# Kernel tuning notes

Hardware: AMD Instinct MI355X
Metric: run time of the kernel (lower is better)

## Reference

```python
import jax, jax.numpy as jnp
import numpy as np

N_TASK = 50000
N_EDGE = 50000
E = 500000
F_TASK = 64
F_EDGE = 64
H = 256
OUT = 256


def _lin(key, fan_in, fan_out):
    kw, kb = jax.random.split(key)
    lim = 1.0 / np.sqrt(fan_in)
    W = jax.random.uniform(kw, (fan_in, fan_out), minval=-lim, maxval=lim, dtype=jnp.float32)
    b = jax.random.uniform(kb, (fan_out,), minval=-lim, maxval=lim, dtype=jnp.float32)
    return W, b


def setup_inputs() -> dict:
    key = jax.random.key(0)
    ks = jax.random.split(key, 20)
    inp = {}
    inp['task_features'] = jax.random.normal(ks[0], (N_TASK, F_TASK), dtype=jnp.float32)
    inp['edge_features'] = jax.random.normal(ks[1], (N_EDGE, F_EDGE), dtype=jnp.float32)
    inp['queue_edges'] = jax.random.randint(ks[2], (2, E), 0, N_TASK)
    inp['type_edges'] = jax.random.randint(ks[3], (2, E), 0, N_TASK)
    inp['affinity_edges'] = jax.random.randint(ks[4], (2, E), 0, N_TASK)  # src<num_tasks, tgt<num_edges
    inp['topology_edges'] = jax.random.randint(ks[5], (2, E), 0, N_EDGE)
    inp['te_w1'], inp['te_b1'] = _lin(ks[6], F_TASK, H)
    inp['te_w2'], inp['te_b2'] = _lin(ks[7], H, H)
    inp['ee_w1'], inp['ee_b1'] = _lin(ks[8], F_EDGE, H)
    inp['ee_w2'], inp['ee_b2'] = _lin(ks[9], H, H)
    inp['gnn_w0'], inp['gnn_b0'] = _lin(ks[10], H, H)
    inp['gnn_w1'], inp['gnn_b1'] = _lin(ks[11], H, H)
    inp['ta_w'], inp['ta_b'] = _lin(ks[12], H, H)
    inp['ea_w'], inp['ea_b'] = _lin(ks[13], H, H)
    inp['out_w1'], inp['out_b1'] = _lin(ks[14], 2 * H, H)
    inp['out_w2'], inp['out_b2'] = _lin(ks[15], H, OUT)
    return inp


def _mean_msg(src_emb, src, tgt, num_segments):
    # scatter-add messages from src nodes into tgt slots, divide by in-degree (clamped >=1)
    msgs = jax.ops.segment_sum(src_emb[src], tgt, num_segments=num_segments)
    cnt = jax.ops.segment_sum(jnp.ones_like(src, dtype=src_emb.dtype), tgt, num_segments=num_segments)
    return msgs / jnp.maximum(cnt, 1.0)[:, None]


def _forward(task_features, edge_features, queue_edges, type_edges, affinity_edges, topology_edges,
             te_w1, te_b1, te_w2, te_b2, ee_w1, ee_b1, ee_w2, ee_b2,
             gnn_w0, gnn_b0, gnn_w1, gnn_b1, ta_w, ta_b, ea_w, ea_b,
             out_w1, out_b1, out_w2, out_b2):
    relu = jax.nn.relu
    # node encoders (Linear-ReLU-Linear-ReLU)
    t = relu(relu(task_features @ te_w1 + te_b1) @ te_w2 + te_b2)   # [N_task, H]
    e = relu(relu(edge_features @ ee_w1 + ee_b1) @ ee_w2 + ee_b2)   # [N_edge, H]

    # queue convolution: messages computed ONCE from original t (torch code never updates task_embeddings in loop)
    qs, qt = queue_edges[0], queue_edges[1]
    q_msgs = jax.ops.segment_sum(t[qs], qt, num_segments=t.shape[0])
    h = t
    for W, b in ((gnn_w0, gnn_b0), (gnn_w1, gnn_b1)):
        h = relu((h + 0.5 * q_msgs) @ W + b)
    t = h

    # type convolution: mean-aggregated same-type messages
    t = t + 0.3 * _mean_msg(t, type_edges[0], type_edges[1], t.shape[0])

    # affinity convolution: bipartite task<->edge exchange (simultaneous update)
    asrc, atgt = affinity_edges[0], affinity_edges[1]
    t_msgs = jax.ops.segment_sum(e[atgt], asrc, num_segments=t.shape[0])
    t_cnt = jax.ops.segment_sum(jnp.ones((asrc.shape[0],), t.dtype), asrc, num_segments=t.shape[0])
    e_msgs = jax.ops.segment_sum(t[asrc], atgt, num_segments=e.shape[0])
    e_cnt = jax.ops.segment_sum(jnp.ones((atgt.shape[0],), e.dtype), atgt, num_segments=e.shape[0])
    t_new = t + 0.3 * t_msgs / jnp.maximum(t_cnt, 1.0)[:, None]
    e_new = e + 0.3 * e_msgs / jnp.maximum(e_cnt, 1.0)[:, None]
    t, e = t_new, e_new

    # topology convolution: edge-edge mean aggregation
    e = e + 0.3 * _mean_msg(e, topology_edges[0], topology_edges[1], e.shape[0])

    # graph-level aggregation
    t_agg = relu(jnp.mean(t, axis=0) @ ta_w + ta_b)  # [H]
    e_agg = relu(jnp.mean(e, axis=0) @ ea_w + ea_b)  # [H]
    combined = jnp.concatenate([t_agg, e_agg], axis=0)  # [2H]
    out = relu(combined @ out_w1 + out_b1) @ out_w2 + out_b2  # [OUT]
    return out


def reference(task_features, edge_features, queue_edges, type_edges, affinity_edges, topology_edges,
              te_w1, te_b1, te_w2, te_b2, ee_w1, ee_b1, ee_w2, ee_b2,
              gnn_w0, gnn_b0, gnn_w1, gnn_b1, ta_w, ta_b, ea_w, ea_b,
              out_w1, out_b1, out_w2, out_b2):
    return _forward(task_features, edge_features, queue_edges, type_edges, affinity_edges, topology_edges,
                    te_w1, te_b1, te_w2, te_b2, ee_w1, ee_b1, ee_w2, ee_b2,
                    gnn_w0, gnn_b0, gnn_w1, gnn_b1, ta_w, ta_b, ea_w, ea_b,
                    out_w1, out_b1, out_w2, out_b2)
```

## Files before the change

kernel.cpp:

```cpp
#include <hip/hip_runtime.h>

#define H 256
#define NT 50000
#define NEDGE 50000
#define NE 500000

#define NBKT 391
#define NBLK 123
#define CHUNK 4096
#define CAP 2816

typedef __attribute__((ext_vector_type(8))) short short8_t;
typedef __attribute__((ext_vector_type(4))) float f32x4;
typedef unsigned short u16;
typedef unsigned int u32;

__device__ __forceinline__ float b2f(u16 v) { return __uint_as_float((u32)v << 16); }
__device__ __forceinline__ u16 f2b(float f) {
    u32 u = __float_as_uint(f);
    u += 0x7FFFu + ((u >> 16) & 1u);
    return (u16)(u >> 16);
}

__device__ __forceinline__ u32 f2fp8_1(float f) {
    u32 u = __float_as_uint(f);
    u32 s = (u >> 24) & 0x80u;
    float af = fabsf(f);
    if (af >= 448.f) return s | 0x7Eu;
    if (af < 0.015625f) {
        int m = (int)rintf(af * 512.0f);
        return s | (u32)m;
    }
    u32 au = __float_as_uint(af);
    u32 r = au + 0x7FFFFu + ((au >> 20) & 1u);
    int e = (int)(r >> 23) - 127;
    return s | (u32)(((e + 7) << 3) | ((r >> 20) & 7u));
}
__device__ __forceinline__ float fp82f_1(u32 b) {
    u32 s = (b & 0x80u) << 24;
    u32 em = b & 0x7Fu;
    float v;
    if (em >= 8) v = __uint_as_float((((em >> 3) + 120u) << 23) | ((em & 7u) << 20));
    else v = (float)em * 0.001953125f;
    return __uint_as_float(__float_as_uint(v) | s);
}
__device__ __forceinline__ u32 pk4_fp8(float a, float b, float c, float d) {
#if __has_builtin(__builtin_amdgcn_cvt_pk_fp8_f32)
    u32 r = 0;
    r = (u32)__builtin_amdgcn_cvt_pk_fp8_f32(a, b, (int)r, false);
    r = (u32)__builtin_amdgcn_cvt_pk_fp8_f32(c, d, (int)r, true);
    return r;
#else
    return f2fp8_1(a) | (f2fp8_1(b) << 8) | (f2fp8_1(c) << 16) | (f2fp8_1(d) << 24);
#endif
}
__device__ __forceinline__ float4 unpk4_fp8(u32 v) {
#if __has_builtin(__builtin_amdgcn_cvt_pk_f32_fp8)
    auto lo = __builtin_amdgcn_cvt_pk_f32_fp8(v, false);
    auto hi = __builtin_amdgcn_cvt_pk_f32_fp8(v, true);
    return make_float4(lo[0], lo[1], hi[0], hi[1]);
#else
    return make_float4(fp82f_1(v & 255u), fp82f_1((v >> 8) & 255u),
                       fp82f_1((v >> 16) & 255u), fp82f_1(v >> 24));
#endif
}

__device__ __forceinline__ const int* pick_list(
    int l, const int* a, const int* b, const int* c, const int* d, const int* e)
{ return (l == 0) ? a : (l == 1) ? b : (l == 2) ? c : (l == 3) ? d : e; }

template<int K1, bool XF32, bool DUAL>
__global__ __launch_bounds__(256) void fused_mlp(
    const void* __restrict__ XA,
    const u16* __restrict__ W1hA, const u16* __restrict__ W1lA, const float* __restrict__ b1A,
    const u16* __restrict__ W2hA, const u16* __restrict__ W2lA, const float* __restrict__ b2A,
    u16* __restrict__ outA, u32* __restrict__ f8A,
    const void* __restrict__ XB,
    const u16* __restrict__ W1hB, const u16* __restrict__ W1lB, const float* __restrict__ b1B,
    const u16* __restrict__ W2hB, const u16* __restrict__ W2lB, const float* __restrict__ b2B,
    u16* __restrict__ outB, u32* __restrict__ f8B,
    int N, int nA)
{
    __shared__ u16 lds[64 * 256];
    int bid = blockIdx.x;
    const void* X = XA;
    const u16 *W1h = W1hA, *W1l = W1lA, *W2h = W2hA, *W2l = W2lA;
    const float *b1 = b1A, *b2 = b2A;
    u16* out = outA;
    u32* f8 = f8A;
    if (DUAL && bid >= nA) {
        bid -= nA; X = XB;
        W1h = W1hB; W1l = W1lB; b1 = b1B;
        W2h = W2hB; W2l = W2lB; b2 = b2B;
        out = outB; f8 = f8B;
    }
    const int m0 = bid * 64;

    constexpr int RCH = K1 / 8;
    for (int i = threadIdx.x; i < 64 * RCH; i += 256) {
        int r = i / RCH, c8 = i % RCH;
        int gr = m0 + r; if (gr >= N) gr = N - 1;
        uint4 v;
        if (XF32) {
            const float* xf = (const float*)X + (size_t)gr * K1 + c8 * 8;
            float4 a = *(const float4*)xf;
            float4 b = *(const float4*)(xf + 4);
            v.x = (u32)f2b(a.x) | ((u32)f2b(a.y) << 16);
            v.y = (u32)f2b(a.z) | ((u32)f2b(a.w) << 16);
            v.z = (u32)f2b(b.x) | ((u32)f2b(b.y) << 16);
            v.w = (u32)f2b(b.z) | ((u32)f2b(b.w) << 16);
        } else {
            v = *(const uint4*)((const u16*)X + (size_t)gr * K1 + c8 * 8);
        }
        u32 byte = (u32)(r * (K1 * 2) + c8 * 16) ^ (u32)((r & 7) << 4);
        *(uint4*)((char*)lds + byte) = v;
    }
    __syncthreads();

    const int wv = threadIdx.x >> 6, l = threadIdx.x & 63;
    const int li = l & 15, lk = l >> 4;

    f32x4 acc[4][4];
    #pragma unroll
    for (int i = 0; i < 4; i++)
        #pragma unroll
        for (int j = 0; j < 4; j++)
            acc[i][j] = (f32x4){0.f, 0.f, 0.f, 0.f};

    {
        constexpr int KS = K1 / 32;
        short8_t whc[4], wlc[4];
        #pragma unroll
        for (int ni = 0; ni < 4; ni++) {
            const size_t wi = (size_t)((wv * 4 + ni) * KS) * 64 + l;
            whc[ni] = ((const short8_t*)W1h)[wi];
            wlc[ni] = ((const short8_t*)W1l)[wi];
        }
        #pragma unroll
        for (int ks = 0; ks < KS; ks++) {
            short8_t whn[4], wln[4];
            if (ks + 1 < KS) {
                #pragma unroll
                for (int ni = 0; ni < 4; ni++) {
                    const size_t wi = (size_t)((wv * 4 + ni) * KS + ks + 1) * 64 + l;
                    whn[ni] = ((const short8_t*)W1h)[wi];
                    wln[ni] = ((const short8_t*)W1l)[wi];
                }
            }
            short8_t xb[4];
            #pragma unroll
            for (int mi = 0; mi < 4; mi++) {
                int m = mi * 16 + li;
                u32 byte = (u32)(m * (K1 * 2) + (ks * 32 + lk * 8) * 2) ^ (u32)((m & 7) << 4);
                xb[mi] = *(const short8_t*)((const char*)lds + byte);
            }
            __builtin_amdgcn_s_setprio(1);
            #pragma unroll
            for (int ni = 0; ni < 4; ni++)
                #pragma unroll
                for (int mi = 0; mi < 4; mi++) {
                    acc[mi][ni] = __builtin_amdgcn_mfma_f32_16x16x32_bf16(wlc[ni], xb[mi], acc[mi][ni], 0, 0, 0);
                    acc[mi][ni] = __builtin_amdgcn_mfma_f32_16x16x32_bf16(whc[ni], xb[mi], acc[mi][ni], 0, 0, 0);
                }
            __builtin_amdgcn_s_setprio(0);
            if (ks + 1 < KS) {
                #pragma unroll
                for (int ni = 0; ni < 4; ni++) { whc[ni] = whn[ni]; wlc[ni] = wln[ni]; }
            }
        }
    }

    __syncthreads();

    #pragma unroll
    for (int ni = 0; ni < 4; ni++) {
        int c = wv * 64 + ni * 16 + lk * 4;
        float4 b4 = *(const float4*)(b1 + c);
        #pragma unroll
        for (int mi = 0; mi < 4; mi++) {
            int m = mi * 16 + li;
            float o0 = fmaxf(acc[mi][ni][0] + b4.x, 0.f);
            float o1 = fmaxf(acc[mi][ni][1] + b4.y, 0.f);
            float o2 = fmaxf(acc[mi][ni][2] + b4.z, 0.f);
            float o3 = fmaxf(acc[mi][ni][3] + b4.w, 0.f);
            u32 w0 = (u32)f2b(o0) | ((u32)f2b(o1) << 16);
            u32 w1 = (u32)f2b(o2) | ((u32)f2b(o3) << 16);
            u32 byte = (u32)(m * 512 + c * 2) ^ (u32)((m & 7) << 4);
            *(uint2*)((char*)lds + byte) = make_uint2(w0, w1);
        }
    }
    __syncthreads();

    #pragma unroll
    for (int i = 0; i < 4; i++)
        #pragma unroll
        for (int j = 0; j < 4; j++)
            acc[i][j] = (f32x4){0.f, 0.f, 0.f, 0.f};

    {
        short8_t whc[4], wlc[4];
        #pragma unroll
        for (int ni = 0; ni < 4; ni++) {
            const size_t wi = (size_t)((wv * 4 + ni) * 8) * 64 + l;
            whc[ni] = ((const short8_t*)W2h)[wi];
            wlc[ni] = ((const short8_t*)W2l)[wi];
        }
        #pragma unroll
        for (int ks = 0; ks < 8; ks++) {
            short8_t whn[4], wln[4];
            if (ks + 1 < 8) {
                #pragma unroll
                for (int ni = 0; ni < 4; ni++) {
                    const size_t wi = (size_t)((wv * 4 + ni) * 8 + ks + 1) * 64 + l;
                    whn[ni] = ((const short8_t*)W2h)[wi];
                    wln[ni] = ((const short8_t*)W2l)[wi];
                }
            }
            short8_t xb[4];
            #pragma unroll
            for (int mi = 0; mi < 4; mi++) {
                int m = mi * 16 + li;
                u32 byte = (u32)(m * 512 + (ks * 32 + lk * 8) * 2) ^ (u32)((m & 7) << 4);
                xb[mi] = *(const short8_t*)((const char*)lds + byte);
            }
            __builtin_amdgcn_s_setprio(1);
            #pragma unroll
            for (int ni = 0; ni < 4; ni++)
                #pragma unroll
                for (int mi = 0; mi < 4; mi++) {
                    acc[mi][ni] = __builtin_amdgcn_mfma_f32_16x16x32_bf16(wlc[ni], xb[mi], acc[mi][ni], 0, 0, 0);
                    acc[mi][ni] = __builtin_amdgcn_mfma_f32_16x16x32_bf16(whc[ni], xb[mi], acc[mi][ni], 0, 0, 0);
                }
            __builtin_amdgcn_s_setprio(0);
            if (ks + 1 < 8) {
                #pragma unroll
                for (int ni = 0; ni < 4; ni++) { whc[ni] = whn[ni]; wlc[ni] = wln[ni]; }
            }
        }
    }

    #pragma unroll
    for (int mi = 0; mi < 4; mi++) {
        int m = m0 + mi * 16 + li;
        if (m < N) {
            #pragma unroll
            for (int ni = 0; ni < 4; ni++) {
                int c = wv * 64 + ni * 16 + lk * 4;
                float4 b4 = *(const float4*)(b2 + c);
                float o0 = fmaxf(acc[mi][ni][0] + b4.x, 0.f);
                float o1 = fmaxf(acc[mi][ni][1] + b4.y, 0.f);
                float o2 = fmaxf(acc[mi][ni][2] + b4.z, 0.f);
                float o3 = fmaxf(acc[mi][ni][3] + b4.w, 0.f);
                u32 w0 = (u32)f2b(o0) | ((u32)f2b(o1) << 16);
                u32 w1 = (u32)f2b(o2) | ((u32)f2b(o3) << 16);
                *(uint2*)(out + (size_t)m * H + c) = make_uint2(w0, w1);
                if (f8) f8[(size_t)m * 64 + (c >> 2)] = pk4_fp8(o0, o1, o2, o3);
            }
        }
    }
}

__global__ __launch_bounds__(256) void gnn_fused(
    const u16* __restrict__ T, const u32* __restrict__ M0,
    const int* __restrict__ csr, const int* __restrict__ off,
    const u16* __restrict__ W1h, const u16* __restrict__ W1l, const float* __restrict__ b1,
    const u16* __restrict__ W2h, const u16* __restrict__ W2l, const float* __restrict__ b2,
    u16* __restrict__ out, u32* __restrict__ f8, int N)
{
    __shared__ u16 ldsX[64 * 256];
    __shared__ u16 ldsS[64 * 256];
    const int wv = threadIdx.x >> 6, l = threadIdx.x & 63;
    const int li = l & 15, lk = l >> 4;
    const int m0 = blockIdx.x * 64;

    for (int rr = 0; rr < 16; rr++) {
        int r = wv * 16 + rr;
        int gr = m0 + r; if (gr >= N) gr = N - 1;
        int o0 = off[gr];
        int d  = off[gr + 1] - o0;
        float4 acc = {0.f, 0.f, 0.f, 0.f};
        int j = 0;
        for (; j + 8 <= d; j += 8) {
            u32 w[8];
            #pragma unroll
            for (int q = 0; q < 8; q++)
                w[q] = M0[(size_t)csr[o0 + j + q] * 64 + l];
            #pragma unroll
            for (int q = 0; q < 8; q++) {
                float4 f = unpk4_fp8(w[q]);
                acc.x += f.x; acc.y += f.y; acc.z += f.z; acc.w += f.w;
            }
        }
        for (; j < d; j++) {
            float4 f = unpk4_fp8(M0[(size_t)csr[o0 + j] * 64 + l]);
            acc.x += f.x; acc.y += f.y; acc.z += f.z; acc.w += f.w;
        }
        ushort4 t4 = ((const ushort4*)(T + (size_t)gr * H))[l];
        u32 s0 = (u32)f2b(acc.x) | ((u32)f2b(acc.y) << 16);
        u32 s1 = (u32)f2b(acc.z) | ((u32)f2b(acc.w) << 16);
        u32 f0 = (u32)f2b(fmaf(0.5f, acc.x, b2f(t4.x)))
               | ((u32)f2b(fmaf(0.5f, acc.y, b2f(t4.y))) << 16);
        u32 f1 = (u32)f2b(fmaf(0.5f, acc.z, b2f(t4.z)))
               | ((u32)f2b(fmaf(0.5f, acc.w, b2f(t4.w))) << 16);
        u32 byte = (u32)(r * 512 + l * 8) ^ (u32)((r & 7) << 4);
        *(uint2*)((char*)ldsX + byte) = make_uint2(f0, f1);
        *(uint2*)((char*)ldsS + byte) = make_uint2(s0, s1);
    }
    __syncthreads();

    f32x4 acc[4][4];
    #pragma unroll
    for (int i = 0; i < 4; i++)
        #pragma unroll
        for (int j = 0; j < 4; j++)
            acc[i][j] = (f32x4){0.f, 0.f, 0.f, 0.f};

    {
        short8_t whc[4], wlc[4];
        #pragma unroll
        for (int ni = 0; ni < 4; ni++) {
            const size_t wi = (size_t)((wv * 4 + ni) * 8) * 64 + l;
            whc[ni] = ((const short8_t*)W1h)[wi];
            wlc[ni] = ((const short8_t*)W1l)[wi];
        }
        #pragma unroll
        for (int ks = 0; ks < 8; ks++) {
            short8_t whn[4], wln[4];
            if (ks + 1 < 8) {
                #pragma unroll
                for (int ni = 0; ni < 4; ni++) {
                    const size_t wi = (size_t)((wv * 4 + ni) * 8 + ks + 1) * 64 + l;
                    whn[ni] = ((const short8_t*)W1h)[wi];
                    wln[ni] = ((const short8_t*)W1l)[wi];
                }
            }
            short8_t xb[4];
            #pragma unroll
            for (int mi = 0; mi < 4; mi++) {
                int m = mi * 16 + li;
                u32 byte = (u32)(m * 512 + (ks * 32 + lk * 8) * 2) ^ (u32)((m & 7) << 4);
                xb[mi] = *(const short8_t*)((const char*)ldsX + byte);
            }
            __builtin_amdgcn_s_setprio(1);
            #pragma unroll
            for (int ni = 0; ni < 4; ni++)
                #pragma unroll
                for (int mi = 0; mi < 4; mi++) {
                    acc[mi][ni] = __builtin_amdgcn_mfma_f32_16x16x32_bf16(wlc[ni], xb[mi], acc[mi][ni], 0, 0, 0);
                    acc[mi][ni] = __builtin_amdgcn_mfma_f32_16x16x32_bf16(whc[ni], xb[mi], acc[mi][ni], 0, 0, 0);
                }
            __builtin_amdgcn_s_setprio(0);
            if (ks + 1 < 8) {
                #pragma unroll
                for (int ni = 0; ni < 4; ni++) { whc[ni] = whn[ni]; wlc[ni] = wln[ni]; }
            }
        }
    }

    __syncthreads();

    #pragma unroll
    for (int ni = 0; ni < 4; ni++) {
        int c = wv * 64 + ni * 16 + lk * 4;
        float4 b4 = *(const float4*)(b1 + c);
        #pragma unroll
        for (int mi = 0; mi < 4; mi++) {
            int m = mi * 16 + li;
            u32 byte = (u32)(m * 512 + c * 2) ^ (u32)((m & 7) << 4);
            uint2 sv = *(const uint2*)((const char*)ldsS + byte);
            float o0 = fmaxf(acc[mi][ni][0] + b4.x, 0.f);
            float o1 = fmaxf(acc[mi][ni][1] + b4.y, 0.f);
            float o2 = fmaxf(acc[mi][ni][2] + b4.z, 0.f);
            float o3 = fmaxf(acc[mi][ni][3] + b4.w, 0.f);
            o0 = fmaf(0.5f, b2f((u16)(sv.x & 0xFFFF)), o0);
            o1 = fmaf(0.5f, b2f((u16)(sv.x >> 16)), o1);
            o2 = fmaf(0.5f, b2f((u16)(sv.y & 0xFFFF)), o2);
            o3 = fmaf(0.5f, b2f((u16)(sv.y >> 16)), o3);
            u32 w0 = (u32)f2b(o0) | ((u32)f2b(o1) << 16);
            u32 w1 = (u32)f2b(o2) | ((u32)f2b(o3) << 16);
            *(uint2*)((char*)ldsX + byte) = make_uint2(w0, w1);
        }
    }
    __syncthreads();

    #pragma unroll
    for (int i = 0; i < 4; i++)
        #pragma unroll
        for (int j = 0; j < 4; j++)
            acc[i][j] = (f32x4){0.f, 0.f, 0.f, 0.f};

    {
        short8_t whc[4], wlc[4];
        #pragma unroll
        for (int ni = 0; ni < 4; ni++) {
            const size_t wi = (size_t)((wv * 4 + ni) * 8) * 64 + l;
            whc[ni] = ((const short8_t*)W2h)[wi];
            wlc[ni] = ((const short8_t*)W2l)[wi];
        }
        #pragma unroll
        for (int ks = 0; ks < 8; ks++) {
            short8_t whn[4], wln[4];
            if (ks + 1 < 8) {
                #pragma unroll
                for (int ni = 0; ni < 4; ni++) {
                    const size_t wi = (size_t)((wv * 4 + ni) * 8 + ks + 1) * 64 + l;
                    whn[ni] = ((const short8_t*)W2h)[wi];
                    wln[ni] = ((const short8_t*)W2l)[wi];
                }
            }
            short8_t xb[4];
            #pragma unroll
            for (int mi = 0; mi < 4; mi++) {
                int m = mi * 16 + li;
                u32 byte = (u32)(m * 512 + (ks * 32 + lk * 8) * 2) ^ (u32)((m & 7) << 4);
                xb[mi] = *(const short8_t*)((const char*)ldsX + byte);
            }
            __builtin_amdgcn_s_setprio(1);
            #pragma unroll
            for (int ni = 0; ni < 4; ni++)
                #pragma unroll
                for (int mi = 0; mi < 4; mi++) {
                    acc[mi][ni] = __builtin_amdgcn_mfma_f32_16x16x32_bf16(wlc[ni], xb[mi], acc[mi][ni], 0, 0, 0);
                    acc[mi][ni] = __builtin_amdgcn_mfma_f32_16x16x32_bf16(whc[ni], xb[mi], acc[mi][ni], 0, 0, 0);
                }
            __builtin_amdgcn_s_setprio(0);
            if (ks + 1 < 8) {
                #pragma unroll
                for (int ni = 0; ni < 4; ni++) { whc[ni] = whn[ni]; wlc[ni] = wln[ni]; }
            }
        }
    }

    #pragma unroll
    for (int mi = 0; mi < 4; mi++) {
        int m = m0 + mi * 16 + li;
        if (m < N) {
            #pragma unroll
            for (int ni = 0; ni < 4; ni++) {
                int c = wv * 64 + ni * 16 + lk * 4;
                float4 b4 = *(const float4*)(b2 + c);
                float o0 = fmaxf(acc[mi][ni][0] + b4.x, 0.f);
                float o1 = fmaxf(acc[mi][ni][1] + b4.y, 0.f);
                float o2 = fmaxf(acc[mi][ni][2] + b4.z, 0.f);
                float o3 = fmaxf(acc[mi][ni][3] + b4.w, 0.f);
                u32 w0 = (u32)f2b(o0) | ((u32)f2b(o1) << 16);
                u32 w1 = (u32)f2b(o2) | ((u32)f2b(o3) << 16);
                *(uint2*)(out + (size_t)m * H + c) = make_uint2(w0, w1);
                if (f8) f8[(size_t)m * 64 + (c >> 2)] = pk4_fp8(o0, o1, o2, o3);
            }
        }
    }
}

__global__ __launch_bounds__(256) void wt_pack(
    const float* __restrict__ s0, const float* __restrict__ s1,
    const float* __restrict__ s2, const float* __restrict__ s3,
    const float* __restrict__ s4, const float* __restrict__ s5,
    u16* __restrict__ arena)
{
    const int li = blockIdx.y;
    const int K = (li == 0 || li == 4) ? 64 : 256;
    const int offs[6] = {0, 32768, 163840, 294912, 425984, 458752};
    int n = K * 256;
    int i = blockIdx.x * 256 + threadIdx.x;
    if (i >= n) return;
    const float* W = (li == 0) ? s0 : (li == 1) ? s1 : (li == 2) ? s2
                   : (li == 3) ? s3 : (li == 4) ? s4 : s5;
    u16* hi = arena + offs[li];
    u16* lo = hi + n;
    int k = i >> 8, c = i & 255;
    float u = W[i];
    u32 b = __float_as_uint(u);
    float r = u - __uint_as_float(b & 0xFFFF0000u);
    int lane = ((k >> 3) & 3) * 16 + (c & 15);
    size_t idx = ((size_t)((c >> 4) * (K >> 5) + (k >> 5)) * 64 + lane) * 8 + (k & 7);
    hi[idx] = (u16)(b >> 16);
    lo[idx] = f2b(r);
}

__global__ __launch_bounds__(256) void hist_kernel(
    const int* __restrict__ k0, const int* __restrict__ k1, const int* __restrict__ k2,
    const int* __restrict__ k3, const int* __restrict__ k4, int* __restrict__ counts)
{
    __shared__ int h[NBKT];
    int l = blockIdx.y;
    const int* k = pick_list(l, k0, k1, k2, k3, k4);
    for (int i = threadIdx.x; i < NBKT; i += 256) h[i] = 0;
    __syncthreads();
    int e0 = blockIdx.x * CHUNK;
    for (int i = threadIdx.x; i < CHUNK; i += 256) {
        int e = e0 + i;
        if (e < NE) atomicAdd(&h[k[e] >> 7], 1);
    }
    __syncthreads();
    int* out = counts + ((size_t)l * NBLK + blockIdx.x) * NBKT;
    for (int i = threadIdx.x; i < NBKT; i += 256) out[i] = h[i];
}

__global__ __launch_bounds__(256) void scan_buckets(
    const int* __restrict__ counts, int* __restrict__ starts, int* __restrict__ bases)
{
    __shared__ int buf[256];
    int l = blockIdx.x, t = threadIdx.x;
    const int* cl = counts + (size_t)l * NBLK * NBKT;
    int* sl = starts + (size_t)l * NBLK * NBKT;
    int b0 = t * 2;
    int totloc[2];
    int s = 0;
    #pragma unroll
    for (int j = 0; j < 2; j++) {
        int b = b0 + j, v = 0;
        if (b < NBKT) for (int k = 0; k < NBLK; k++) v += cl[k * NBKT + b];
        totloc[j] = v; s += v;
    }
    buf[t] = s; __syncthreads();
    for (int st = 1; st < 256; st <<= 1) {
        int v = (t >= st) ? buf[t - st] : 0; __syncthreads();
        buf[t] += v; __syncthreads();
    }
    int run = buf[t] - s;
    #pragma unroll
    for (int j = 0; j < 2; j++) {
        int b = b0 + j;
        if (b < NBKT) {
            bases[l * (NBKT + 1) + b] = run;
            int p = run;
            for (int k = 0; k < NBLK; k++) { sl[k * NBKT + b] = p; p += cl[k * NBKT + b]; }
            run += totloc[j];
        }
    }
    if (t == 255) bases[l * (NBKT + 1) + NBKT] = NE;
}

__global__ __launch_bounds__(256) void partition_kernel(
    const int* __restrict__ k0, const int* __restrict__ k1, const int* __restrict__ k2,
    const int* __restrict__ k3, const int* __restrict__ k4,
    const int* __restrict__ v0, const int* __restrict__ v1, const int* __restrict__ v2,
    const int* __restrict__ v3, const int* __restrict__ v4,
    const int* __restrict__ starts, int* __restrict__ csr)
{
    __shared__ u32 ent[CHUNK];
    __shared__ u16 ebk[CHUNK];
    __shared__ int cnt[NBKT], loff[NBKT], cur[NBKT], gst[NBKT];
    __shared__ int buf[256];
    int l = blockIdx.y, t = threadIdx.x;
    const int* k = pick_list(l, k0, k1, k2, k3, k4);
    const int* v = pick_list(l, v0, v1, v2, v3, v4);
    const int* st = starts + ((size_t)l * NBLK + blockIdx.x) * NBKT;
    for (int i = t; i < NBKT; i += 256) { cnt[i] = 0; gst[i] = st[i]; }
    __syncthreads();
    int e0 = blockIdx.x * CHUNK;
    u32 ep[16]; int eb[16];
    #pragma unroll
    for (int j = 0; j < 16; j++) {
        int e = e0 + j * 256 + t;
        if (e < NE) {
            int key = k[e];
            eb[j] = key >> 7;
            ep[j] = ((u32)(key & 127) << 16) | (u32)v[e];
            atomicAdd(&cnt[eb[j]], 1);
        } else eb[j] = -1;
    }
    __syncthreads();
    int b0 = t * 2;
    int c0 = (b0 < NBKT) ? cnt[b0] : 0;
    int c1 = (b0 + 1 < NBKT) ? cnt[b0 + 1] : 0;
    int s = c0 + c1;
    buf[t] = s; __syncthreads();
    for (int stp = 1; stp < 256; stp <<= 1) {
        int x = (t >= stp) ? buf[t - stp] : 0; __syncthreads();
        buf[t] += x; __syncthreads();
    }
    int run = buf[t] - s;
    if (b0 < NBKT)     { loff[b0] = run;          cur[b0] = run; }
    if (b0 + 1 < NBKT) { loff[b0 + 1] = run + c0; cur[b0 + 1] = run + c0; }
    __syncthreads();
    #pragma unroll
    for (int j = 0; j < 16; j++) {
        if (eb[j] >= 0) {
            int p = atomicAdd(&cur[eb[j]], 1);
            ent[p] = ep[j]; ebk[p] = (u16)eb[j];
        }
    }
    __syncthreads();
    int nv = min(CHUNK, NE - e0);
    int* c = csr + (size_t)l * NE;
    for (int i = t; i < nv; i += 256) {
        int b = ebk[i];
        c[gst[b] + (i - loff[b])] = (int)ent[i];
    }
}

__global__ __launch_bounds__(256) void bucket_csr(
    const int* __restrict__ bases, int* __restrict__ csr, int* __restrict__ off)
{
    __shared__ int seg[CAP];
    __shared__ int hist[128], scn[128];
    int l = blockIdx.y, b = blockIdx.x, t = threadIdx.x;
    int base = bases[l * (NBKT + 1) + b];
    int end  = bases[l * (NBKT + 1) + b + 1];
    int sz = end - base; if (sz > CAP) sz = CAP;
    int* c = csr + (size_t)l * NE;
    for (int i = t; i < sz; i += 256) seg[i] = c[base + i];
    if (t < 128) hist[t] = 0;
    __syncthreads();
    for (int i = t; i < sz; i += 256) atomicAdd(&hist[seg[i] >> 16], 1);
    __syncthreads();
    if (t < 128) scn[t] = hist[t];
    __syncthreads();
    for (int st = 1; st < 128; st <<= 1) {
        int v = 0;
        if (t < 128 && t >= st) v = scn[t - st];
        __syncthreads();
        if (t < 128) scn[t] += v;
        __syncthreads();
    }
    if (t < 128) {
        int key = b * 128 + t;
        int excl = scn[t] - hist[t];
        if (key < NT) off[l * (NT + 1) + key] = base + excl;
        hist[t] = excl;
    }
    if (b == 0 && t == 128) off[l * (NT + 1) + NT] = NE;
    __syncthreads();
    for (int i = t; i < sz; i += 256) {
        int u = seg[i];
        int p = atomicAdd(&hist[u >> 16], 1);
        c[base + p] = u & 0xFFFF;
    }
}

__global__ __launch_bounds__(256) void gather_mean_f8(
    const u32* __restrict__ srcA, const int* __restrict__ csrA, const int* __restrict__ offA,
    const u16* __restrict__ baseA, u16* __restrict__ dstA, u32* __restrict__ m8A,
    const u32* __restrict__ srcB, const int* __restrict__ csrB, const int* __restrict__ offB,
    const u16* __restrict__ baseB, u16* __restrict__ dstB, u32* __restrict__ m8B,
    float alpha, int nA, int N)
{
    int bid = blockIdx.x;
    const u32* src = srcA; const int* csr = csrA; const int* off = offA;
    const u16* base = baseA; u16* dst = dstA; u32* m8 = m8A;
    if (bid >= nA) {
        bid -= nA; src = srcB; csr = csrB; off = offB; base = baseB; dst = dstB; m8 = m8B;
    }
    int r = (bid * 256 + threadIdx.x) >> 6;
    int lane = threadIdx.x & 63;
    if (r >= N) return;
    int o0 = off[r];
    int d  = off[r + 1] - o0;
    float4 acc = {0.f, 0.f, 0.f, 0.f};
    int j = 0;
    for (; j + 8 <= d; j += 8) {
        u32 w[8];
        #pragma unroll
        for (int q = 0; q < 8; q++)
            w[q] = src[(size_t)csr[o0 + j + q] * 64 + lane];
        #pragma unroll
        for (int q = 0; q < 8; q++) {
            float4 f = unpk4_fp8(w[q]);
            acc.x += f.x; acc.y += f.y; acc.z += f.z; acc.w += f.w;
        }
    }
    for (; j < d; j++) {
        float4 f = unpk4_fp8(src[(size_t)csr[o0 + j] * 64 + lane]);
        acc.x += f.x; acc.y += f.y; acc.z += f.z; acc.w += f.w;
    }
    float s = alpha / (float)max(d, 1);
    ushort4 b = ((const ushort4*)(base + (size_t)r * H))[lane];
    float o0f = fmaf(s, acc.x, b2f(b.x));
    float o1f = fmaf(s, acc.y, b2f(b.y));
    float o2f = fmaf(s, acc.z, b2f(b.z));
    float o3f = fmaf(s, acc.w, b2f(b.w));
    ushort4 pk;
    pk.x = f2b(o0f); pk.y = f2b(o1f); pk.z = f2b(o2f); pk.w = f2b(o3f);
    ((ushort4*)(dst + (size_t)r * H))[lane] = pk;
    if (m8) m8[(size_t)r * 64 + lane] = pk4_fp8(o0f, o1f, o2f, o3f);
}

__global__ __launch_bounds__(256) void colsum_slots(
    const u16* __restrict__ embA, const u16* __restrict__ embB,
    float* __restrict__ part, int N)
{
    int blk = blockIdx.x;
    const u16* emb = (blk < 256) ? embA : embB;
    int rb = blk & 255;
    int c = threadIdx.x;
    float s = 0.f;
    for (int r = rb; r < N; r += 256)
        s += b2f(emb[(size_t)r * H + c]);
    part[(size_t)blk * H + c] = s;
}

__global__ __launch_bounds__(256) void final_mlp(
    const float* __restrict__ part, float invNT, float invNE,
    const float* __restrict__ ta_w, const float* __restrict__ ta_b,
    const float* __restrict__ ea_w, const float* __restrict__ ea_b,
    const float* __restrict__ ow1, const float* __restrict__ ob1,
    const float* __restrict__ ow2, const float* __restrict__ ob2,
    float* __restrict__ out)
{
    __shared__ float tm[H], em[H], comb[2 * H], hid[H];
    int t = threadIdx.x;
    float st = 0.f, se = 0.f;
    for (int b = 0; b < 256; b++) {
        st += part[(size_t)b * H + t];
        se += part[(size_t)(256 + b) * H + t];
    }
    tm[t] = st * invNT;
    em[t] = se * invNE;
    __syncthreads();
    float s = ta_b[t];
    for (int k = 0; k < H; k++) s += tm[k] * ta_w[k * H + t];
    comb[t] = fmaxf(s, 0.f);
    s = ea_b[t];
    for (int k = 0; k < H; k++) s += em[k] * ea_w[k * H + t];
    comb[H + t] = fmaxf(s, 0.f);
    __syncthreads();
    s = ob1[t];
    for (int k = 0; k < 2 * H; k++) s += comb[k] * ow1[k * H + t];
    hid[t] = fmaxf(s, 0.f);
    __syncthreads();
    s = ob2[t];
    for (int k = 0; k < H; k++) s += hid[k] * ow2[k * H + t];
    out[t] = s;
}

extern "C" void kernel_launch(void* const* d_in, const int* in_sizes, int n_in,
                              void* d_out, int out_size, void* d_ws, size_t ws_size,
                              hipStream_t stream) {
    const float* tf  = (const float*)d_in[0];
    const float* ef  = (const float*)d_in[1];
    const int*   qe  = (const int*)d_in[2];
    const int*   te  = (const int*)d_in[3];
    const int*   ae  = (const int*)d_in[4];
    const int*   pe  = (const int*)d_in[5];
    const float* te_w1 = (const float*)d_in[6];  const float* te_b1 = (const float*)d_in[7];
    const float* te_w2 = (const float*)d_in[8];  const float* te_b2 = (const float*)d_in[9];
    const float* ee_w1 = (const float*)d_in[10]; const float* ee_b1 = (const float*)d_in[11];
    const float* ee_w2 = (const float*)d_in[12]; const float* ee_b2 = (const float*)d_in[13];
    const float* gw0 = (const float*)d_in[14];   const float* gb0 = (const float*)d_in[15];
    const float* gw1 = (const float*)d_in[16];   const float* gb1 = (const float*)d_in[17];
    const float* ta_w = (const float*)d_in[18];  const float* ta_b = (const float*)d_in[19];
    const float* ea_w = (const float*)d_in[20];  const float* ea_b = (const float*)d_in[21];
    const float* ow1 = (const float*)d_in[22];   const float* ob1 = (const float*)d_in[23];
    const float* ow2 = (const float*)d_in[24];   const float* ob2 = (const float*)d_in[25];

    const size_t NB = (size_t)NT * H;
    u16* T  = (u16*)d_ws;
    u16* Bf = T + NB;
    u16* S  = Bf + NB;
    u16* F  = S + NB;
    float* sumpad = (float*)(F + NB);
    int* off5   = (int*)(sumpad + 2 * H);
    int* csr5   = off5 + 5 * (NT + 1);
    int* counts = csr5 + (size_t)5 * NE;
    int* starts = counts + (size_t)5 * NBLK * NBKT;
    int* bases  = starts + (size_t)5 * NBLK * NBKT;
    u16* arena = (u16*)(((size_t)counts + 15) & ~(size_t)15);
    u16* wt_te1_h = arena + 0;      u16* wt_te1_l = arena + 16384;
    u16* wt_te2_h = arena + 32768;  u16* wt_te2_l = arena + 98304;
    u16* wt_g0_h  = arena + 163840; u16* wt_g0_l  = arena + 229376;
    u16* wt_g1_h  = arena + 294912; u16* wt_g1_l  = arena + 360448;
    u16* wt_ee1_h = arena + 425984; u16* wt_ee1_l = arena + 442368;
    u16* wt_ee2_h = arena + 458752; u16* wt_ee2_l = arena + 524288;
    u32* M0 = (u32*)(((size_t)(bases + 5 * (NBKT + 1)) + 15) & ~(size_t)15);
    u32* M1 = M0 + NB / 4;
    u32* M2 = M1 + NB / 4;
    u32* M3 = M2 + NB / 4;
    u32* M4 = M3 + NB / 4;
    float* part = (float*)(M4 + NB / 4);

    const int MG = (NT + 63) / 64;
    const int GB = (NT * 64) / 256;

    const int *k0 = qe + NE, *k1 = te + NE, *k2 = ae,      *k3 = ae + NE, *k4 = pe + NE;
    const int *v0 = qe,      *v1 = te,      *v2 = ae + NE, *v3 = ae,      *v4 = pe;

    dim3 pg(NBLK, 5);
    hist_kernel<<<pg, 256, 0, stream>>>(k0, k1, k2, k3, k4, counts);
    scan_buckets<<<5, 256, 0, stream>>>(counts, starts, bases);
    partition_kernel<<<pg, 256, 0, stream>>>(k0, k1, k2, k3, k4, v0, v1, v2, v3, v4,
                                             starts, csr5);
    wt_pack<<<dim3(256, 6), 256, 0, stream>>>(te_w1, te_w2, gw0, gw1, ee_w1, ee_w2, arena);
    bucket_csr<<<dim3(NBKT, 5), 256, 0, stream>>>(bases, csr5, off5);

    #define LOFF(l) (off5 + (l) * (NT + 1))
    #define LCSR(l) (csr5 + (size_t)(l) * NE)

    fused_mlp<64, true, true><<<2 * MG, 256, 0, stream>>>(
        tf, wt_te1_h, wt_te1_l, te_b1, wt_te2_h, wt_te2_l, te_b2, T, M0,
        ef, wt_ee1_h, wt_ee1_l, ee_b1, wt_ee2_h, wt_ee2_l, ee_b2, Bf, M2,
        NT, MG);

    gnn_fused<<<MG, 256, 0, stream>>>(
        T, M0, LCSR(0), LOFF(0),
        wt_g0_h, wt_g0_l, gb0, wt_g1_h, wt_g1_l, gb1, T, M1, NT);

    gather_mean_f8<<<GB, 256, 0, stream>>>(
        M1, LCSR(1), LOFF(1), T, F, M3,
        M1, LCSR(1), LOFF(1), T, F, M3,
        0.3f, GB, NT);

    gather_mean_f8<<<2 * GB, 256, 0, stream>>>(
        M2, LCSR(2), LOFF(2), F, S, nullptr,
        M3, LCSR(3), LOFF(3), Bf, T, M4,
        0.3f, GB, NT);

    gather_mean_f8<<<GB, 256, 0, stream>>>(
        M4, LCSR(4), LOFF(4), T, Bf, nullptr,
        M4, LCSR(4), LOFF(4), T, Bf, nullptr,
        0.3f, GB, NT);

    colsum_slots<<<512, 256, 0, stream>>>(S, Bf, part, NT);
    final_mlp<<<1, 256, 0, stream>>>(part, 1.f / NT, 1.f / NEDGE,
                                     ta_w, ta_b, ea_w, ea_b, ow1, ob1, ow2, ob2,
                                     (float*)d_out);
}
```

Measured before the change: 497.6 us.

## Co-schedule encoder MLPs with CSR build kernels and restructure GNN gather stages

The task and edge encoder MLPs now run as extra blocks inside the partition and bucket-CSR kernels, so encoder compute overlaps the memory-bound CSR construction. The GNN queue step is split into a standalone gather followed by a generic fused MLP that adds the scaled residual in its first epilogue. The type and affinity gathers are merged into one kernel that reads T once and writes both outputs. Weight packing moves to a separate workspace region. This cuts launches and overlaps phases, at the cost of larger shared-memory arenas and heterogeneous blocks within one launch.

```diff
diff --git a/kernel.cpp b/kernel.cpp
--- a/kernel.cpp
+++ b/kernel.cpp
@@ -69,49 +69,326 @@
     int l, const int* a, const int* b, const int* c, const int* d, const int* e)
 { return (l == 0) ? a : (l == 1) ? b : (l == 2) ? c : (l == 3) ? d : e; }
 
-template<int K1, bool XF32, bool DUAL>
+__device__ __forceinline__ void enc_body(
+    char* arena, int bid, const float* __restrict__ X,
+    const u16* __restrict__ W1h, const u16* __restrict__ W1l, const float* __restrict__ b1,
+    const u16* __restrict__ W2h, const u16* __restrict__ W2l, const float* __restrict__ b2,
+    u16* __restrict__ out, u32* __restrict__ f8, int N)
+{
+    const int m0 = bid * 64;
+
+    for (int i = threadIdx.x; i < 64 * 8; i += 256) {
+        int r = i >> 3, c8 = i & 7;
+        int gr = m0 + r; if (gr >= N) gr = N - 1;
+        const float* xf = X + (size_t)gr * 64 + c8 * 8;
+        float4 a = *(const float4*)xf;
+        float4 b = *(const float4*)(xf + 4);
+        uint4 v;
+        v.x = (u32)f2b(a.x) | ((u32)f2b(a.y) << 16);
+        v.y = (u32)f2b(a.z) | ((u32)f2b(a.w) << 16);
+        v.z = (u32)f2b(b.x) | ((u32)f2b(b.y) << 16);
+        v.w = (u32)f2b(b.z) | ((u32)f2b(b.w) << 16);
+        u32 byte = (u32)(r * 128 + c8 * 16) ^ (u32)((r & 7) << 4);
+        *(uint4*)(arena + byte) = v;
+    }
+    __syncthreads();
+
+    const int wv = threadIdx.x >> 6, l = threadIdx.x & 63;
+    const int li = l & 15, lk = l >> 4;
+
+    f32x4 acc[4][4];
+    #pragma unroll
+    for (int i = 0; i < 4; i++)
+        #pragma unroll
+        for (int j = 0; j < 4; j++)
+            acc[i][j] = (f32x4){0.f, 0.f, 0.f, 0.f};
+
+    {
+        short8_t whc[4], wlc[4];
+        #pragma unroll
+        for (int ni = 0; ni < 4; ni++) {
+            const size_t wi = (size_t)((wv * 4 + ni) * 2) * 64 + l;
+            whc[ni] = ((const short8_t*)W1h)[wi];
+            wlc[ni] = ((const short8_t*)W1l)[wi];
+        }
+        #pragma unroll
+        for (int ks = 0; ks < 2; ks++) {
+            short8_t whn[4], wln[4];
+            if (ks + 1 < 2) {
+                #pragma unroll
+                for (int ni = 0; ni < 4; ni++) {
+                    const size_t wi = (size_t)((wv * 4 + ni) * 2 + ks + 1) * 64 + l;
+                    whn[ni] = ((const short8_t*)W1h)[wi];
+                    wln[ni] = ((const short8_t*)W1l)[wi];
+                }
+            }
+            short8_t xb[4];
+            #pragma unroll
+            for (int mi = 0; mi < 4; mi++) {
+                int m = mi * 16 + li;
+                u32 byte = (u32)(m * 128 + (ks * 32 + lk * 8) * 2) ^ (u32)((m & 7) << 4);
+                xb[mi] = *(const short8_t*)(arena + byte);
+            }
+            __builtin_amdgcn_s_setprio(1);
+            #pragma unroll
+            for (int ni = 0; ni < 4; ni++)
+                #pragma unroll
+                for (int mi = 0; mi < 4; mi++) {
+                    acc[mi][ni] = __builtin_amdgcn_mfma_f32_16x16x32_bf16(wlc[ni], xb[mi], acc[mi][ni], 0, 0, 0);
+                    acc[mi][ni] = __builtin_amdgcn_mfma_f32_16x16x32_bf16(whc[ni], xb[mi], acc[mi][ni], 0, 0, 0);
+                }
+            __builtin_amdgcn_s_setprio(0);
+            if (ks + 1 < 2) {
+                #pragma unroll
+                for (int ni = 0; ni < 4; ni++) { whc[ni] = whn[ni]; wlc[ni] = wln[ni]; }
+            }
+        }
+    }
+
+    __syncthreads();
+
+    #pragma unroll
+    for (int ni = 0; ni < 4; ni++) {
+        int c = wv * 64 + ni * 16 + lk * 4;
+        float4 b4 = *(const float4*)(b1 + c);
+        #pragma unroll
+        for (int mi = 0; mi < 4; mi++) {
+            int m = mi * 16 + li;
+            float o0 = fmaxf(acc[mi][ni][0] + b4.x, 0.f);
+            float o1 = fmaxf(acc[mi][ni][1] + b4.y, 0.f);
+            float o2 = fmaxf(acc[mi][ni][2] + b4.z, 0.f);
+            float o3 = fmaxf(acc[mi][ni][3] + b4.w, 0.f);
+            u32 w0 = (u32)f2b(o0) | ((u32)f2b(o1) << 16);
+            u32 w1 = (u32)f2b(o2) | ((u32)f2b(o3) << 16);
+            u32 byte = (u32)(m * 512 + c * 2) ^ (u32)((m & 7) << 4);
+            *(uint2*)(arena + byte) = make_uint2(w0, w1);
+        }
+    }
+    __syncthreads();
+
+    #pragma unroll
+    for (int i = 0; i < 4; i++)
+        #pragma unroll
+        for (int j = 0; j < 4; j++)
+            acc[i][j] = (f32x4){0.f, 0.f, 0.f, 0.f};
+
+    {
+        short8_t whc[4], wlc[4];
+        #pragma unroll
+        for (int ni = 0; ni < 4; ni++) {
+            const size_t wi = (size_t)((wv * 4 + ni) * 8) * 64 + l;
+            whc[ni] = ((const short8_t*)W2h)[wi];
+            wlc[ni] = ((const short8_t*)W2l)[wi];
+        }
+        #pragma unroll
+        for (int ks = 0; ks < 8; ks++) {
+            short8_t whn[4], wln[4];
+            if (ks + 1 < 8) {
+                #pragma unroll
+                for (int ni = 0; ni < 4; ni++) {
+                    const size_t wi = (size_t)((wv * 4 + ni) * 8 + ks + 1) * 64 + l;
+                    whn[ni] = ((const short8_t*)W2h)[wi];
+                    wln[ni] = ((const short8_t*)W2l)[wi];
+                }
+            }
+            short8_t xb[4];
+            #pragma unroll
+            for (int mi = 0; mi < 4; mi++) {
+                int m = mi * 16 + li;
+                u32 byte = (u32)(m * 512 + (ks * 32 + lk * 8) * 2) ^ (u32)((m & 7) << 4);
+                xb[mi] = *(const short8_t*)(arena + byte);
+            }
+            __builtin_amdgcn_s_setprio(1);
+            #pragma unroll
+            for (int ni = 0; ni < 4; ni++)
+                #pragma unroll
+                for (int mi = 0; mi < 4; mi++) {
+                    acc[mi][ni] = __builtin_amdgcn_mfma_f32_16x16x32_bf16(wlc[ni], xb[mi], acc[mi][ni], 0, 0, 0);
+                    acc[mi][ni] = __builtin_amdgcn_mfma_f32_16x16x32_bf16(whc[ni], xb[mi], acc[mi][ni], 0, 0, 0);
+                }
+            __builtin_amdgcn_s_setprio(0);
+            if (ks + 1 < 8) {
+                #pragma unroll
+                for (int ni = 0; ni < 4; ni++) { whc[ni] = whn[ni]; wlc[ni] = wln[ni]; }
+            }
+        }
+    }
+
+    __syncthreads();
+    #pragma unroll
+    for (int ni = 0; ni < 4; ni++) {
+        int c = wv * 64 + ni * 16 + lk * 4;
+        float4 b4 = *(const float4*)(b2 + c);
+        #pragma unroll
+        for (int mi = 0; mi < 4; mi++) {
+            int m = mi * 16 + li;
+            float o0 = fmaxf(acc[mi][ni][0] + b4.x, 0.f);
+            float o1 = fmaxf(acc[mi][ni][1] + b4.y, 0.f);
+            float o2 = fmaxf(acc[mi][ni][2] + b4.z, 0.f);
+            float o3 = fmaxf(acc[mi][ni][3] + b4.w, 0.f);
+            u32 w0 = (u32)f2b(o0) | ((u32)f2b(o1) << 16);
+            u32 w1 = (u32)f2b(o2) | ((u32)f2b(o3) << 16);
+            u32 byte = (u32)(m * 512 + c * 2) ^ (u32)((m & 7) << 4);
+            *(uint2*)(arena + byte) = make_uint2(w0, w1);
+        }
+    }
+    __syncthreads();
+    for (int i = threadIdx.x; i < 64 * 32; i += 256) {
+        int r = i >> 5, c8 = i & 31;
+        int m = m0 + r;
+        if (m < N) {
+            u32 byte = (u32)(r * 512 + c8 * 16) ^ (u32)((r & 7) << 4);
+            uint4 v = *(const uint4*)(arena + byte);
+            *(uint4*)(out + (size_t)m * H + c8 * 8) = v;
+            u32 p0 = pk4_fp8(b2f((u16)(v.x & 0xFFFF)), b2f((u16)(v.x >> 16)),
+                             b2f((u16)(v.y & 0xFFFF)), b2f((u16)(v.y >> 16)));
+            u32 p1 = pk4_fp8(b2f((u16)(v.z & 0xFFFF)), b2f((u16)(v.z >> 16)),
+                             b2f((u16)(v.w & 0xFFFF)), b2f((u16)(v.w >> 16)));
+            *(uint2*)(f8 + (size_t)m * 64 + c8 * 2) = make_uint2(p0, p1);
+        }
+    }
+}
+
+__global__ __launch_bounds__(256) void part_enc(
+    const int* __restrict__ k0, const int* __restrict__ k1, const int* __restrict__ k2,
+    const int* __restrict__ k3, const int* __restrict__ k4,
+    const int* __restrict__ v0, const int* __restrict__ v1, const int* __restrict__ v2,
+    const int* __restrict__ v3, const int* __restrict__ v4,
+    const int* __restrict__ starts, int* __restrict__ csr,
+    const float* __restrict__ X,
+    const u16* __restrict__ W1h, const u16* __restrict__ W1l, const float* __restrict__ b1,
+    const u16* __restrict__ W2h, const u16* __restrict__ W2l, const float* __restrict__ b2,
+    u16* __restrict__ out, u32* __restrict__ f8, int N, int nCSR)
+{
+    __shared__ char arena[32768];
+    if ((int)blockIdx.x >= nCSR) {
+        enc_body(arena, blockIdx.x - nCSR, X, W1h, W1l, b1, W2h, W2l, b2, out, f8, N);
+        return;
+    }
+    u32* ent = (u32*)arena;
+    u16* ebk = (u16*)(arena + 16384);
+    int* cnt  = (int*)(arena + 24576);
+    int* loff = cnt + NBKT;
+    int* cur  = loff + NBKT;
+    int* gst  = cur + NBKT;
+    int* buf  = (int*)(arena + 24576 + 4 * 4 * NBKT);
+    int p = blockIdx.x;
+    int l = p / NBLK, blk = p % NBLK;
+    int t = threadIdx.x;
+    const int* k = pick_list(l, k0, k1, k2, k3, k4);
+    const int* v = pick_list(l, v0, v1, v2, v3, v4);
+    const int* st = starts + ((size_t)l * NBLK + blk) * NBKT;
+    for (int i = t; i < NBKT; i += 256) { cnt[i] = 0; gst[i] = st[i]; }
+    __syncthreads();
+    int e0 = blk * CHUNK;
+    u32 ep[16]; int eb[16];
+    #pragma unroll
+    for (int j = 0; j < 16; j++) {
+        int e = e0 + j * 256 + t;
+        if (e < NE) {
+            int key = k[e];
+            eb[j] = key >> 7;
+            ep[j] = ((u32)(key & 127) << 16) | (u32)v[e];
+            atomicAdd(&cnt[eb[j]], 1);
+        } else eb[j] = -1;
+    }
+    __syncthreads();
+    int b0 = t * 2;
+    int c0 = (b0 < NBKT) ? cnt[b0] : 0;
+    int c1 = (b0 + 1 < NBKT) ? cnt[b0 + 1] : 0;
+    int s = c0 + c1;
+    buf[t] = s; __syncthreads();
+    for (int stp = 1; stp < 256; stp <<= 1) {
+        int x = (t >= stp) ? buf[t - stp] : 0; __syncthreads();
+        buf[t] += x; __syncthreads();
+    }
+    int run = buf[t] - s;
+    if (b0 < NBKT)     { loff[b0] = run;          cur[b0] = run; }
+    if (b0 + 1 < NBKT) { loff[b0 + 1] = run + c0; cur[b0 + 1] = run + c0; }
+    __syncthreads();
+    #pragma unroll
+    for (int j = 0; j < 16; j++) {
+        if (eb[j] >= 0) {
+            int q = atomicAdd(&cur[eb[j]], 1);
+            ent[q] = ep[j]; ebk[q] = (u16)eb[j];
+        }
+    }
+    __syncthreads();
+    int nv = min(CHUNK, NE - e0);
+    int* c = csr + (size_t)l * NE;
+    for (int i = t; i < nv; i += 256) {
+        int b = ebk[i];
+        c[gst[b] + (i - loff[b])] = (int)ent[i];
+    }
+}
+
+__global__ __launch_bounds__(256) void buck_enc(
+    const int* __restrict__ bases, int* __restrict__ csr, int* __restrict__ off,
+    const float* __restrict__ X,
+    const u16* __restrict__ W1h, const u16* __restrict__ W1l, const float* __restrict__ b1,
+    const u16* __restrict__ W2h, const u16* __restrict__ W2l, const float* __restrict__ b2,
+    u16* __restrict__ out, u32* __restrict__ f8, int N, int nCSR)
+{
+    __shared__ char arena[32768];
+    if ((int)blockIdx.x >= nCSR) {
+        enc_body(arena, blockIdx.x - nCSR, X, W1h, W1l, b1, W2h, W2l, b2, out, f8, N);
+        return;
+    }
+    int* seg  = (int*)arena;
+    int* hist = (int*)(arena + 11264);
+    int* scn  = hist + 128;
+    int p = blockIdx.x;
+    int l = p / NBKT, b = p % NBKT;
+    int t = threadIdx.x;
+    int base = bases[l * (NBKT + 1) + b];
+    int end  = bases[l * (NBKT + 1) + b + 1];
+    int sz = end - base; if (sz > CAP) sz = CAP;
+    int* c = csr + (size_t)l * NE;
+    for (int i = t; i < sz; i += 256) seg[i] = c[base + i];
+    if (t < 128) hist[t] = 0;
+    __syncthreads();
+    for (int i = t; i < sz; i += 256) atomicAdd(&hist[seg[i] >> 16], 1);
+    __syncthreads();
+    if (t < 128) scn[t] = hist[t];
+    __syncthreads();
+    for (int st = 1; st < 128; st <<= 1) {
+        int v = 0;
+        if (t < 128 && t >= st) v = scn[t - st];
+        __syncthreads();
+        if (t < 128) scn[t] += v;
+        __syncthreads();
+    }
+    if (t < 128) {
+        int key = b * 128 + t;
+        int excl = scn[t] - hist[t];
+        if (key < NT) off[l * (NT + 1) + key] = base + excl;
+        hist[t] = excl;
+    }
+    if (b == 0 && t == 128) off[l * (NT + 1) + NT] = NE;
+    __syncthreads();
+    for (int i = t; i < sz; i += 256) {
+        int u = seg[i];
+        int q = atomicAdd(&hist[u >> 16], 1);
+        c[base + q] = u & 0xFFFF;
+    }
+}
+
+template<int K1>
 __global__ __launch_bounds__(256) void fused_mlp(
-    const void* __restrict__ XA,
-    const u16* __restrict__ W1hA, const u16* __restrict__ W1lA, const float* __restrict__ b1A,
-    const u16* __restrict__ W2hA, const u16* __restrict__ W2lA, const float* __restrict__ b2A,
-    u16* __restrict__ outA, u32* __restrict__ f8A,
-    const void* __restrict__ XB,
-    const u16* __restrict__ W1hB, const u16* __restrict__ W1lB, const float* __restrict__ b1B,
-    const u16* __restrict__ W2hB, const u16* __restrict__ W2lB, const float* __restrict__ b2B,
-    u16* __restrict__ outB, u32* __restrict__ f8B,
-    int N, int nA)
+    const u16* __restrict__ X, const u16* __restrict__ Q,
+    const u16* __restrict__ W1h, const u16* __restrict__ W1l, const float* __restrict__ b1,
+    const u16* __restrict__ W2h, const u16* __restrict__ W2l, const float* __restrict__ b2,
+    u16* __restrict__ out, u32* __restrict__ f8,
+    int N, float s2)
 {
     __shared__ u16 lds[64 * 256];
-    int bid = blockIdx.x;
-    const void* X = XA;
-    const u16 *W1h = W1hA, *W1l = W1lA, *W2h = W2hA, *W2l = W2lA;
-    const float *b1 = b1A, *b2 = b2A;
-    u16* out = outA;
-    u32* f8 = f8A;
-    if (DUAL && bid >= nA) {
-        bid -= nA; X = XB;
-        W1h = W1hB; W1l = W1lB; b1 = b1B;
-        W2h = W2hB; W2l = W2lB; b2 = b2B;
-        out = outB; f8 = f8B;
-    }
-    const int m0 = bid * 64;
+    const int m0 = blockIdx.x * 64;
 
     constexpr int RCH = K1 / 8;
     for (int i = threadIdx.x; i < 64 * RCH; i += 256) {
         int r = i / RCH, c8 = i % RCH;
         int gr = m0 + r; if (gr >= N) gr = N - 1;
-        uint4 v;
-        if (XF32) {
-            const float* xf = (const float*)X + (size_t)gr * K1 + c8 * 8;
-            float4 a = *(const float4*)xf;
-            float4 b = *(const float4*)(xf + 4);
-            v.x = (u32)f2b(a.x) | ((u32)f2b(a.y) << 16);
-            v.y = (u32)f2b(a.z) | ((u32)f2b(a.w) << 16);
-            v.z = (u32)f2b(b.x) | ((u32)f2b(b.y) << 16);
-            v.w = (u32)f2b(b.z) | ((u32)f2b(b.w) << 16);
-        } else {
-            v = *(const uint4*)((const u16*)X + (size_t)gr * K1 + c8 * 8);
-        }
+        uint4 v = *(const uint4*)(X + (size_t)gr * K1 + c8 * 8);
         u32 byte = (u32)(r * (K1 * 2) + c8 * 16) ^ (u32)((r & 7) << 4);
         *(uint4*)((char*)lds + byte) = v;
     }
@@ -176,6 +453,80 @@
     for (int ni = 0; ni < 4; ni++) {
         int c = wv * 64 + ni * 16 + lk * 4;
         float4 b4 = *(const float4*)(b1 + c);
+        #pragma unroll
+        for (int mi = 0; mi < 4; mi++) {
+            int m = mi * 16 + li;
+            float o0 = fmaxf(acc[mi][ni][0] + b4.x, 0.f);
+            float o1 = fmaxf(acc[mi][ni][1] + b4.y, 0.f);
+            float o2 = fmaxf(acc[mi][ni][2] + b4.z, 0.f);
+            float o3 = fmaxf(acc[mi][ni][3] + b4.w, 0.f);
+            int gm = m0 + m; if (gm >= N) gm = N - 1;
+            uint2 qv = *(const uint2*)(Q + (size_t)gm * 256 + c);
+            o0 = fmaf(s2, b2f((u16)(qv.x & 0xFFFF)), o0);
+            o1 = fmaf(s2, b2f((u16)(qv.x >> 16)), o1);
+            o2 = fmaf(s2, b2f((u16)(qv.y & 0xFFFF)), o2);
+            o3 = fmaf(s2, b2f((u16)(qv.y >> 16)), o3);
+            u32 w0 = (u32)f2b(o0) | ((u32)f2b(o1) << 16);
+            u32 w1 = (u32)f2b(o2) | ((u32)f2b(o3) << 16);
+            u32 byte = (u32)(m * 512 + c * 2) ^ (u32)((m & 7) << 4);
+            *(uint2*)((char*)lds + byte) = make_uint2(w0, w1);
+        }
+    }
+    __syncthreads();
+
+    #pragma unroll
+    for (int i = 0; i < 4; i++)
+        #pragma unroll
+        for (int j = 0; j < 4; j++)
+            acc[i][j] = (f32x4){0.f, 0.f, 0.f, 0.f};
+
+    {
+        short8_t whc[4], wlc[4];
+        #pragma unroll
+        for (int ni = 0; ni < 4; ni++) {
+            const size_t wi = (size_t)((wv * 4 + ni) * 8) * 64 + l;
+            whc[ni] = ((const short8_t*)W2h)[wi];
+            wlc[ni] = ((const short8_t*)W2l)[wi];
+        }
+        #pragma unroll
+        for (int ks = 0; ks < 8; ks++) {
+            short8_t whn[4], wln[4];
+            if (ks + 1 < 8) {
+                #pragma unroll
+                for (int ni = 0; ni < 4; ni++) {
+                    const size_t wi = (size_t)((wv * 4 + ni) * 8 + ks + 1) * 64 + l;
+                    whn[ni] = ((const short8_t*)W2h)[wi];
+                    wln[ni] = ((const short8_t*)W2l)[wi];
+                }
+            }
+            short8_t xb[4];
+            #pragma unroll
+            for (int mi = 0; mi < 4; mi++) {
+                int m = mi * 16 + li;
+                u32 byte = (u32)(m * 512 + (ks * 32 + lk * 8) * 2) ^ (u32)((m & 7) << 4);
+                xb[mi] = *(const short8_t*)((const char*)lds + byte);
+            }
+            __builtin_amdgcn_s_setprio(1);
+            #pragma unroll
+            for (int ni = 0; ni < 4; ni++)
+                #pragma unroll
+                for (int mi = 0; mi < 4; mi++) {
+                    acc[mi][ni] = __builtin_amdgcn_mfma_f32_16x16x32_bf16(wlc[ni], xb[mi], acc[mi][ni], 0, 0, 0);
+                    acc[mi][ni] = __builtin_amdgcn_mfma_f32_16x16x32_bf16(whc[ni], xb[mi], acc[mi][ni], 0, 0, 0);
+                }
+            __builtin_amdgcn_s_setprio(0);
+            if (ks + 1 < 8) {
+                #pragma unroll
+                for (int ni = 0; ni < 4; ni++) { whc[ni] = whn[ni]; wlc[ni] = wln[ni]; }
+            }
+        }
+    }
+
+    __syncthreads();
+    #pragma unroll
+    for (int ni = 0; ni < 4; ni++) {
+        int c = wv * 64 + ni * 16 + lk * 4;
+        float4 b4 = *(const float4*)(b2 + c);
         #pragma unroll
         for (int mi = 0; mi < 4; mi++) {
             int m = mi * 16 + li;
@@ -190,264 +541,18 @@
         }
     }
     __syncthreads();
-
-    #pragma unroll
-    for (int i = 0; i < 4; i++)
-        #pragma unroll
-        for (int j = 0; j < 4; j++)
-            acc[i][j] = (f32x4){0.f, 0.f, 0.f, 0.f};
-
-    {
-        short8_t whc[4], wlc[4];
-        #pragma unroll
-        for (int ni = 0; ni < 4; ni++) {
-            const size_t wi = (size_t)((wv * 4 + ni) * 8) * 64 + l;
-            whc[ni] = ((const short8_t*)W2h)[wi];
-            wlc[ni] = ((const short8_t*)W2l)[wi];
-        }
-        #pragma unroll
-        for (int ks = 0; ks < 8; ks++) {
-            short8_t whn[4], wln[4];
-            if (ks + 1 < 8) {
-                #pragma unroll
-                for (int ni = 0; ni < 4; ni++) {
-                    const size_t wi = (size_t)((wv * 4 + ni) * 8 + ks + 1) * 64 + l;
-                    whn[ni] = ((const short8_t*)W2h)[wi];
-                    wln[ni] = ((const short8_t*)W2l)[wi];
-                }
-            }
-            short8_t xb[4];
-            #pragma unroll
-            for (int mi = 0; mi < 4; mi++) {
-                int m = mi * 16 + li;
-                u32 byte = (u32)(m * 512 + (ks * 32 + lk * 8) * 2) ^ (u32)((m & 7) << 4);
-                xb[mi] = *(const short8_t*)((const char*)lds + byte);
-            }
-            __builtin_amdgcn_s_setprio(1);
-            #pragma unroll
-            for (int ni = 0; ni < 4; ni++)
-                #pragma unroll
-                for (int mi = 0; mi < 4; mi++) {
-                    acc[mi][ni] = __builtin_amdgcn_mfma_f32_16x16x32_bf16(wlc[ni], xb[mi], acc[mi][ni], 0, 0, 0);
-                    acc[mi][ni] = __builtin_amdgcn_mfma_f32_16x16x32_bf16(whc[ni], xb[mi], acc[mi][ni], 0, 0, 0);
-                }
-            __builtin_amdgcn_s_setprio(0);
-            if (ks + 1 < 8) {
-                #pragma unroll
-                for (int ni = 0; ni < 4; ni++) { whc[ni] = whn[ni]; wlc[ni] = wln[ni]; }
-            }
-        }
-    }
-
-    #pragma unroll
-    for (int mi = 0; mi < 4; mi++) {
-        int m = m0 + mi * 16 + li;
+    for (int i = threadIdx.x; i < 64 * 32; i += 256) {
+        int r = i >> 5, c8 = i & 31;
+        int m = m0 + r;
         if (m < N) {
-            #pragma unroll
-            for (int ni = 0; ni < 4; ni++) {
-                int c = wv * 64 + ni * 16 + lk * 4;
-                float4 b4 = *(const float4*)(b2 + c);
-                float o0 = fmaxf(acc[mi][ni][0] + b4.x, 0.f);
-                float o1 = fmaxf(acc[mi][ni][1] + b4.y, 0.f);
-                float o2 = fmaxf(acc[mi][ni][2] + b4.z, 0.f);
-                float o3 = fmaxf(acc[mi][ni][3] + b4.w, 0.f);
-                u32 w0 = (u32)f2b(o0) | ((u32)f2b(o1) << 16);
-                u32 w1 = (u32)f2b(o2) | ((u32)f2b(o3) << 16);
-                *(uint2*)(out + (size_t)m * H + c) = make_uint2(w0, w1);
-                if (f8) f8[(size_t)m * 64 + (c >> 2)] = pk4_fp8(o0, o1, o2, o3);
-            }
-        }
-    }
-}
-
-__global__ __launch_bounds__(256) void gnn_fused(
-    const u16* __restrict__ T, const u32* __restrict__ M0,
-    const int* __restrict__ csr, const int* __restrict__ off,
-    const u16* __restrict__ W1h, const u16* __restrict__ W1l, const float* __restrict__ b1,
-    const u16* __restrict__ W2h, const u16* __restrict__ W2l, const float* __restrict__ b2,
-    u16* __restrict__ out, u32* __restrict__ f8, int N)
-{
-    __shared__ u16 ldsX[64 * 256];
-    __shared__ u16 ldsS[64 * 256];
-    const int wv = threadIdx.x >> 6, l = threadIdx.x & 63;
-    const int li = l & 15, lk = l >> 4;
-    const int m0 = blockIdx.x * 64;
-
-    for (int rr = 0; rr < 16; rr++) {
-        int r = wv * 16 + rr;
-        int gr = m0 + r; if (gr >= N) gr = N - 1;
-        int o0 = off[gr];
-        int d  = off[gr + 1] - o0;
-        float4 acc = {0.f, 0.f, 0.f, 0.f};
-        int j = 0;
-        for (; j + 8 <= d; j += 8) {
-            u32 w[8];
-            #pragma unroll
-            for (int q = 0; q < 8; q++)
-                w[q] = M0[(size_t)csr[o0 + j + q] * 64 + l];
-            #pragma unroll
-            for (int q = 0; q < 8; q++) {
-                float4 f = unpk4_fp8(w[q]);
-                acc.x += f.x; acc.y += f.y; acc.z += f.z; acc.w += f.w;
-            }
-        }
-        for (; j < d; j++) {
-            float4 f = unpk4_fp8(M0[(size_t)csr[o0 + j] * 64 + l]);
-            acc.x += f.x; acc.y += f.y; acc.z += f.z; acc.w += f.w;
-        }
-        ushort4 t4 = ((const ushort4*)(T + (size_t)gr * H))[l];
-        u32 s0 = (u32)f2b(acc.x) | ((u32)f2b(acc.y) << 16);
-        u32 s1 = (u32)f2b(acc.z) | ((u32)f2b(acc.w) << 16);
-        u32 f0 = (u32)f2b(fmaf(0.5f, acc.x, b2f(t4.x)))
-               | ((u32)f2b(fmaf(0.5f, acc.y, b2f(t4.y))) << 16);
-        u32 f1 = (u32)f2b(fmaf(0.5f, acc.z, b2f(t4.z)))
-               | ((u32)f2b(fmaf(0.5f, acc.w, b2f(t4.w))) << 16);
-        u32 byte = (u32)(r * 512 + l * 8) ^ (u32)((r & 7) << 4);
-        *(uint2*)((char*)ldsX + byte) = make_uint2(f0, f1);
-        *(uint2*)((char*)ldsS + byte) = make_uint2(s0, s1);
-    }
-    __syncthreads();
-
-    f32x4 acc[4][4];
-    #pragma unroll
-    for (int i = 0; i < 4; i++)
-        #pragma unroll
-        for (int j = 0; j < 4; j++)
-            acc[i][j] = (f32x4){0.f, 0.f, 0.f, 0.f};
-
-    {
-        short8_t whc[4], wlc[4];
-        #pragma unroll
-        for (int ni = 0; ni < 4; ni++) {
-            const size_t wi = (size_t)((wv * 4 + ni) * 8) * 64 + l;
-            whc[ni] = ((const short8_t*)W1h)[wi];
-            wlc[ni] = ((const short8_t*)W1l)[wi];
-        }
-        #pragma unroll
-        for (int ks = 0; ks < 8; ks++) {
-            short8_t whn[4], wln[4];
-            if (ks + 1 < 8) {
-                #pragma unroll
-                for (int ni = 0; ni < 4; ni++) {
-                    const size_t wi = (size_t)((wv * 4 + ni) * 8 + ks + 1) * 64 + l;
-                    whn[ni] = ((const short8_t*)W1h)[wi];
-                    wln[ni] = ((const short8_t*)W1l)[wi];
-                }
-            }
-            short8_t xb[4];
-            #pragma unroll
-            for (int mi = 0; mi < 4; mi++) {
-                int m = mi * 16 + li;
-                u32 byte = (u32)(m * 512 + (ks * 32 + lk * 8) * 2) ^ (u32)((m & 7) << 4);
-                xb[mi] = *(const short8_t*)((const char*)ldsX + byte);
-            }
-            __builtin_amdgcn_s_setprio(1);
-            #pragma unroll
-            for (int ni = 0; ni < 4; ni++)
-                #pragma unroll
-                for (int mi = 0; mi < 4; mi++) {
-                    acc[mi][ni] = __builtin_amdgcn_mfma_f32_16x16x32_bf16(wlc[ni], xb[mi], acc[mi][ni], 0, 0, 0);
-                    acc[mi][ni] = __builtin_amdgcn_mfma_f32_16x16x32_bf16(whc[ni], xb[mi], acc[mi][ni], 0, 0, 0);
-                }
-            __builtin_amdgcn_s_setprio(0);
-            if (ks + 1 < 8) {
-                #pragma unroll
-                for (int ni = 0; ni < 4; ni++) { whc[ni] = whn[ni]; wlc[ni] = wln[ni]; }
-            }
-        }
-    }
-
-    __syncthreads();
-
-    #pragma unroll
-    for (int ni = 0; ni < 4; ni++) {
-        int c = wv * 64 + ni * 16 + lk * 4;
-        float4 b4 = *(const float4*)(b1 + c);
-        #pragma unroll
-        for (int mi = 0; mi < 4; mi++) {
-            int m = mi * 16 + li;
-            u32 byte = (u32)(m * 512 + c * 2) ^ (u32)((m & 7) << 4);
-            uint2 sv = *(const uint2*)((const char*)ldsS + byte);
-            float o0 = fmaxf(acc[mi][ni][0] + b4.x, 0.f);
-            float o1 = fmaxf(acc[mi][ni][1] + b4.y, 0.f);
-            float o2 = fmaxf(acc[mi][ni][2] + b4.z, 0.f);
-            float o3 = fmaxf(acc[mi][ni][3] + b4.w, 0.f);
-            o0 = fmaf(0.5f, b2f((u16)(sv.x & 0xFFFF)), o0);
-            o1 = fmaf(0.5f, b2f((u16)(sv.x >> 16)), o1);
-            o2 = fmaf(0.5f, b2f((u16)(sv.y & 0xFFFF)), o2);
-            o3 = fmaf(0.5f, b2f((u16)(sv.y >> 16)), o3);
-            u32 w0 = (u32)f2b(o0) | ((u32)f2b(o1) << 16);
-            u32 w1 = (u32)f2b(o2) | ((u32)f2b(o3) << 16);
-            *(uint2*)((char*)ldsX + byte) = make_uint2(w0, w1);
-        }
-    }
-    __syncthreads();
-
-    #pragma unroll
-    for (int i = 0; i < 4; i++)
-        #pragma unroll
-        for (int j = 0; j < 4; j++)
-            acc[i][j] = (f32x4){0.f, 0.f, 0.f, 0.f};
-
-    {
-        short8_t whc[4], wlc[4];
-        #pragma unroll
-        for (int ni = 0; ni < 4; ni++) {
-            const size_t wi = (size_t)((wv * 4 + ni) * 8) * 64 + l;
-            whc[ni] = ((const short8_t*)W2h)[wi];
-            wlc[ni] = ((const short8_t*)W2l)[wi];
-        }
-        #pragma unroll
-        for (int ks = 0; ks < 8; ks++) {
-            short8_t whn[4], wln[4];
-            if (ks + 1 < 8) {
-                #pragma unroll
-                for (int ni = 0; ni < 4; ni++) {
-                    const size_t wi = (size_t)((wv * 4 + ni) * 8 + ks + 1) * 64 + l;
-                    whn[ni] = ((const short8_t*)W2h)[wi];
-                    wln[ni] = ((const short8_t*)W2l)[wi];
-                }
-            }
-            short8_t xb[4];
-            #pragma unroll
-            for (int mi = 0; mi < 4; mi++) {
-                int m = mi * 16 + li;
-                u32 byte = (u32)(m * 512 + (ks * 32 + lk * 8) * 2) ^ (u32)((m & 7) << 4);
-                xb[mi] = *(const short8_t*)((const char*)ldsX + byte);
-            }
-            __builtin_amdgcn_s_setprio(1);
-            #pragma unroll
-            for (int ni = 0; ni < 4; ni++)
-                #pragma unroll
-                for (int mi = 0; mi < 4; mi++) {
-                    acc[mi][ni] = __builtin_amdgcn_mfma_f32_16x16x32_bf16(wlc[ni], xb[mi], acc[mi][ni], 0, 0, 0);
-                    acc[mi][ni] = __builtin_amdgcn_mfma_f32_16x16x32_bf16(whc[ni], xb[mi], acc[mi][ni], 0, 0, 0);
-                }
-            __builtin_amdgcn_s_setprio(0);
-            if (ks + 1 < 8) {
-                #pragma unroll
-                for (int ni = 0; ni < 4; ni++) { whc[ni] = whn[ni]; wlc[ni] = wln[ni]; }
-            }
-        }
-    }
-
-    #pragma unroll
-    for (int mi = 0; mi < 4; mi++) {
-        int m = m0 + mi * 16 + li;
-        if (m < N) {
-            #pragma unroll
-            for (int ni = 0; ni < 4; ni++) {
-                int c = wv * 64 + ni * 16 + lk * 4;
-                float4 b4 = *(const float4*)(b2 + c);
-                float o0 = fmaxf(acc[mi][ni][0] + b4.x, 0.f);
-                float o1 = fmaxf(acc[mi][ni][1] + b4.y, 0.f);
-                float o2 = fmaxf(acc[mi][ni][2] + b4.z, 0.f);
-                float o3 = fmaxf(acc[mi][ni][3] + b4.w, 0.f);
-                u32 w0 = (u32)f2b(o0) | ((u32)f2b(o1) << 16);
-                u32 w1 = (u32)f2b(o2) | ((u32)f2b(o3) << 16);
-                *(uint2*)(out + (size_t)m * H + c) = make_uint2(w0, w1);
-                if (f8) f8[(size_t)m * 64 + (c >> 2)] = pk4_fp8(o0, o1, o2, o3);
-            }
+            u32 byte = (u32)(r * 512 + c8 * 16) ^ (u32)((r & 7) << 4);
+            uint4 v = *(const uint4*)((const char*)lds + byte);
+            *(uint4*)(out + (size_t)m * H + c8 * 8) = v;
+            u32 p0 = pk4_fp8(b2f((u16)(v.x & 0xFFFF)), b2f((u16)(v.x >> 16)),
+                             b2f((u16)(v.y & 0xFFFF)), b2f((u16)(v.y >> 16)));
+            u32 p1 = pk4_fp8(b2f((u16)(v.z & 0xFFFF)), b2f((u16)(v.z >> 16)),
+                             b2f((u16)(v.w & 0xFFFF)), b2f((u16)(v.w >> 16)));
+            *(uint2*)(f8 + (size_t)m * 64 + c8 * 2) = make_uint2(p0, p1);
         }
     }
 }
@@ -532,118 +637,113 @@
     if (t == 255) bases[l * (NBKT + 1) + NBKT] = NE;
 }
 
-__global__ __launch_bounds__(256) void partition_kernel(
-    const int* __restrict__ k0, const int* __restrict__ k1, const int* __restrict__ k2,
-    const int* __restrict__ k3, const int* __restrict__ k4,
-    const int* __restrict__ v0, const int* __restrict__ v1, const int* __restrict__ v2,
-    const int* __restrict__ v3, const int* __restrict__ v4,
-    const int* __restrict__ starts, int* __restrict__ csr)
-{
-    __shared__ u32 ent[CHUNK];
-    __shared__ u16 ebk[CHUNK];
-    __shared__ int cnt[NBKT], loff[NBKT], cur[NBKT], gst[NBKT];
-    __shared__ int buf[256];
-    int l = blockIdx.y, t = threadIdx.x;
-    const int* k = pick_list(l, k0, k1, k2, k3, k4);
-    const int* v = pick_list(l, v0, v1, v2, v3, v4);
-    const int* st = starts + ((size_t)l * NBLK + blockIdx.x) * NBKT;
-    for (int i = t; i < NBKT; i += 256) { cnt[i] = 0; gst[i] = st[i]; }
-    __syncthreads();
-    int e0 = blockIdx.x * CHUNK;
-    u32 ep[16]; int eb[16];
-    #pragma unroll
-    for (int j = 0; j < 16; j++) {
-        int e = e0 + j * 256 + t;
-        if (e < NE) {
-            int key = k[e];
-            eb[j] = key >> 7;
-            ep[j] = ((u32)(key & 127) << 16) | (u32)v[e];
-            atomicAdd(&cnt[eb[j]], 1);
-        } else eb[j] = -1;
-    }
-    __syncthreads();
-    int b0 = t * 2;
-    int c0 = (b0 < NBKT) ? cnt[b0] : 0;
-    int c1 = (b0 + 1 < NBKT) ? cnt[b0 + 1] : 0;
-    int s = c0 + c1;
-    buf[t] = s; __syncthreads();
-    for (int stp = 1; stp < 256; stp <<= 1) {
-        int x = (t >= stp) ? buf[t - stp] : 0; __syncthreads();
-        buf[t] += x; __syncthreads();
-    }
-    int run = buf[t] - s;
-    if (b0 < NBKT)     { loff[b0] = run;          cur[b0] = run; }
-    if (b0 + 1 < NBKT) { loff[b0 + 1] = run + c0; cur[b0 + 1] = run + c0; }
-    __syncthreads();
-    #pragma unroll
-    for (int j = 0; j < 16; j++) {
-        if (eb[j] >= 0) {
-            int p = atomicAdd(&cur[eb[j]], 1);
-            ent[p] = ep[j]; ebk[p] = (u16)eb[j];
-        }
-    }
-    __syncthreads();
-    int nv = min(CHUNK, NE - e0);
-    int* c = csr + (size_t)l * NE;
-    for (int i = t; i < nv; i += 256) {
-        int b = ebk[i];
-        c[gst[b] + (i - loff[b])] = (int)ent[i];
-    }
-}
-
-__global__ __launch_bounds__(256) void bucket_csr(
-    const int* __restrict__ bases, int* __restrict__ csr, int* __restrict__ off)
-{
-    __shared__ int seg[CAP];
-    __shared__ int hist[128], scn[128];
-    int l = blockIdx.y, b = blockIdx.x, t = threadIdx.x;
-    int base = bases[l * (NBKT + 1) + b];
-    int end  = bases[l * (NBKT + 1) + b + 1];
-    int sz = end - base; if (sz > CAP) sz = CAP;
-    int* c = csr + (size_t)l * NE;
-    for (int i = t; i < sz; i += 256) seg[i] = c[base + i];
-    if (t < 128) hist[t] = 0;
-    __syncthreads();
-    for (int i = t; i < sz; i += 256) atomicAdd(&hist[seg[i] >> 16], 1);
-    __syncthreads();
-    if (t < 128) scn[t] = hist[t];
-    __syncthreads();
-    for (int st = 1; st < 128; st <<= 1) {
-        int v = 0;
-        if (t < 128 && t >= st) v = scn[t - st];
-        __syncthreads();
-        if (t < 128) scn[t] += v;
-        __syncthreads();
-    }
-    if (t < 128) {
-        int key = b * 128 + t;
-        int excl = scn[t] - hist[t];
-        if (key < NT) off[l * (NT + 1) + key] = base + excl;
-        hist[t] = excl;
-    }
-    if (b == 0 && t == 128) off[l * (NT + 1) + NT] = NE;
-    __syncthreads();
-    for (int i = t; i < sz; i += 256) {
-        int u = seg[i];
-        int p = atomicAdd(&hist[u >> 16], 1);
-        c[base + p] = u & 0xFFFF;
-    }
+__global__ __launch_bounds__(256) void gather_q_f8(
+    const u32* __restrict__ src, const int* __restrict__ csr,
+    const int* __restrict__ off, const u16* __restrict__ baseT,
+    u16* __restrict__ sumOut, u16* __restrict__ fuseOut, float s2, int N)
+{
+    int r = (blockIdx.x * 256 + threadIdx.x) >> 6;
+    int lane = threadIdx.x & 63;
+    if (r >= N) return;
+    int o0 = off[r];
+    int d  = off[r + 1] - o0;
+    float4 acc = {0.f, 0.f, 0.f, 0.f};
+    int j = 0;
+    for (; j + 8 <= d; j += 8) {
+        u32 w[8];
+        #pragma unroll
+        for (int q = 0; q < 8; q++)
+            w[q] = src[(size_t)csr[o0 + j + q] * 64 + lane];
+        #pragma unroll
+        for (int q = 0; q < 8; q++) {
+            float4 f = unpk4_fp8(w[q]);
+            acc.x += f.x; acc.y += f.y; acc.z += f.z; acc.w += f.w;
+        }
+    }
+    for (; j < d; j++) {
+        float4 f = unpk4_fp8(src[(size_t)csr[o0 + j] * 64 + lane]);
+        acc.x += f.x; acc.y += f.y; acc.z += f.z; acc.w += f.w;
+    }
+    ushort4 pk;
+    pk.x = f2b(acc.x); pk.y = f2b(acc.y); pk.z = f2b(acc.z); pk.w = f2b(acc.w);
+    ((ushort4*)(sumOut + (size_t)r * H))[lane] = pk;
+    ushort4 b = ((const ushort4*)(baseT + (size_t)r * H))[lane];
+    pk.x = f2b(fmaf(s2, acc.x, b2f(b.x)));
+    pk.y = f2b(fmaf(s2, acc.y, b2f(b.y)));
+    pk.z = f2b(fmaf(s2, acc.z, b2f(b.z)));
+    pk.w = f2b(fmaf(s2, acc.w, b2f(b.w)));
+    ((ushort4*)(fuseOut + (size_t)r * H))[lane] = pk;
+}
+
+__global__ __launch_bounds__(256) void gather_task2(
+    const u32* __restrict__ M1s, const int* __restrict__ csr1, const int* __restrict__ off1,
+    const u32* __restrict__ M2s, const int* __restrict__ csr2, const int* __restrict__ off2,
+    const u16* __restrict__ T, u16* __restrict__ Sout, u32* __restrict__ M3out, int N)
+{
+    int r = (blockIdx.x * 256 + threadIdx.x) >> 6;
+    int lane = threadIdx.x & 63;
+    if (r >= N) return;
+
+    float4 a1 = {0.f, 0.f, 0.f, 0.f};
+    {
+        int o0 = off1[r], d = off1[r + 1] - o0;
+        int j = 0;
+        for (; j + 8 <= d; j += 8) {
+            u32 w[8];
+            #pragma unroll
+            for (int q = 0; q < 8; q++)
+                w[q] = M1s[(size_t)csr1[o0 + j + q] * 64 + lane];
+            #pragma unroll
+            for (int q = 0; q < 8; q++) {
+                float4 f = unpk4_fp8(w[q]);
+                a1.x += f.x; a1.y += f.y; a1.z += f.z; a1.w += f.w;
+            }
+        }
+        for (; j < d; j++) {
+            float4 f = unpk4_fp8(M1s[(size_t)csr1[o0 + j] * 64 + lane]);
+            a1.x += f.x; a1.y += f.y; a1.z += f.z; a1.w += f.w;
+        }
+        float s = 0.3f / (float)max(d, 1);
+        a1.x *= s; a1.y *= s; a1.z *= s; a1.w *= s;
+    }
+    float4 a2 = {0.f, 0.f, 0.f, 0.f};
+    {
+        int o0 = off2[r], d = off2[r + 1] - o0;
+        int j = 0;
+        for (; j + 8 <= d; j += 8) {
+            u32 w[8];
+            #pragma unroll
+            for (int q = 0; q < 8; q++)
+                w[q] = M2s[(size_t)csr2[o0 + j + q] * 64 + lane];
+            #pragma unroll
+            for (int q = 0; q < 8; q++) {
+                float4 f = unpk4_fp8(w[q]);
+                a2.x += f.x; a2.y += f.y; a2.z += f.z; a2.w += f.w;
+            }
+        }
+        for (; j < d; j++) {
+            float4 f = unpk4_fp8(M2s[(size_t)csr2[o0 + j] * 64 + lane]);
+            a2.x += f.x; a2.y += f.y; a2.z += f.z; a2.w += f.w;
+        }
+        float s = 0.3f / (float)max(d, 1);
+        a2.x *= s; a2.y *= s; a2.z *= s; a2.w *= s;
+    }
+    ushort4 b = ((const ushort4*)(T + (size_t)r * H))[lane];
+    float f0 = b2f(b.x) + a1.x, f1 = b2f(b.y) + a1.y;
+    float f2 = b2f(b.z) + a1.z, f3 = b2f(b.w) + a1.w;
+    M3out[(size_t)r * 64 + lane] = pk4_fp8(f0, f1, f2, f3);
+    ushort4 pk;
+    pk.x = f2b(f0 + a2.x); pk.y = f2b(f1 + a2.y);
+    pk.z = f2b(f2 + a2.z); pk.w = f2b(f3 + a2.w);
+    ((ushort4*)(Sout + (size_t)r * H))[lane] = pk;
 }
 
 __global__ __launch_bounds__(256) void gather_mean_f8(
-    const u32* __restrict__ srcA, const int* __restrict__ csrA, const int* __restrict__ offA,
-    const u16* __restrict__ baseA, u16* __restrict__ dstA, u32* __restrict__ m8A,
-    const u32* __restrict__ srcB, const int* __restrict__ csrB, const int* __restrict__ offB,
-    const u16* __restrict__ baseB, u16* __restrict__ dstB, u32* __restrict__ m8B,
-    float alpha, int nA, int N)
-{
-    int bid = blockIdx.x;
-    const u32* src = srcA; const int* csr = csrA; const int* off = offA;
-    const u16* base = baseA; u16* dst = dstA; u32* m8 = m8A;
-    if (bid >= nA) {
-        bid -= nA; src = srcB; csr = csrB; off = offB; base = baseB; dst = dstB; m8 = m8B;
-    }
-    int r = (bid * 256 + threadIdx.x) >> 6;
+    const u32* __restrict__ src, const int* __restrict__ csr, const int* __restrict__ off,
+    const u16* __restrict__ base, u16* __restrict__ dst, u32* __restrict__ m8,
+    float alpha, int N)
+{
+    int r = (blockIdx.x * 256 + threadIdx.x) >> 6;
     int lane = threadIdx.x & 63;
     if (r >= N) return;
     int o0 = off[r];
@@ -756,60 +856,56 @@
     int* counts = csr5 + (size_t)5 * NE;
     int* starts = counts + (size_t)5 * NBLK * NBKT;
     int* bases  = starts + (size_t)5 * NBLK * NBKT;
-    u16* arena = (u16*)(((size_t)counts + 15) & ~(size_t)15);
-    u16* wt_te1_h = arena + 0;      u16* wt_te1_l = arena + 16384;
-    u16* wt_te2_h = arena + 32768;  u16* wt_te2_l = arena + 98304;
-    u16* wt_g0_h  = arena + 163840; u16* wt_g0_l  = arena + 229376;
-    u16* wt_g1_h  = arena + 294912; u16* wt_g1_l  = arena + 360448;
-    u16* wt_ee1_h = arena + 425984; u16* wt_ee1_l = arena + 442368;
-    u16* wt_ee2_h = arena + 458752; u16* wt_ee2_l = arena + 524288;
     u32* M0 = (u32*)(((size_t)(bases + 5 * (NBKT + 1)) + 15) & ~(size_t)15);
     u32* M1 = M0 + NB / 4;
     u32* M2 = M1 + NB / 4;
     u32* M3 = M2 + NB / 4;
     u32* M4 = M3 + NB / 4;
     float* part = (float*)(M4 + NB / 4);
+    u16* warena = (u16*)(((size_t)(part + 512 * 256) + 15) & ~(size_t)15);
+    u16* wt_te1_h = warena + 0;      u16* wt_te1_l = warena + 16384;
+    u16* wt_te2_h = warena + 32768;  u16* wt_te2_l = warena + 98304;
+    u16* wt_g0_h  = warena + 163840; u16* wt_g0_l  = warena + 229376;
+    u16* wt_g1_h  = warena + 294912; u16* wt_g1_l  = warena + 360448;
+    u16* wt_ee1_h = warena + 425984; u16* wt_ee1_l = warena + 442368;
+    u16* wt_ee2_h = warena + 458752; u16* wt_ee2_l = warena + 524288;
 
     const int MG = (NT + 63) / 64;
     const int GB = (NT * 64) / 256;
+    const int NPART = NBLK * 5;
+    const int NBUCK = NBKT * 5;
 
     const int *k0 = qe + NE, *k1 = te + NE, *k2 = ae,      *k3 = ae + NE, *k4 = pe + NE;
     const int *v0 = qe,      *v1 = te,      *v2 = ae + NE, *v3 = ae,      *v4 = pe;
 
-    dim3 pg(NBLK, 5);
-    hist_kernel<<<pg, 256, 0, stream>>>(k0, k1, k2, k3, k4, counts);
+    wt_pack<<<dim3(256, 6), 256, 0, stream>>>(te_w1, te_w2, gw0, gw1, ee_w1, ee_w2, warena);
+    hist_kernel<<<dim3(NBLK, 5), 256, 0, stream>>>(k0, k1, k2, k3, k4, counts);
     scan_buckets<<<5, 256, 0, stream>>>(counts, starts, bases);
-    partition_kernel<<<pg, 256, 0, stream>>>(k0, k1, k2, k3, k4, v0, v1, v2, v3, v4,
-                                             starts, csr5);
-    wt_pack<<<dim3(256, 6), 256, 0, stream>>>(te_w1, te_w2, gw0, gw1, ee_w1, ee_w2, arena);
-    bucket_csr<<<dim3(NBKT, 5), 256, 0, stream>>>(bases, csr5, off5);
+
+    part_enc<<<NPART + MG, 256, 0, stream>>>(
+        k0, k1, k2, k3, k4, v0, v1, v2, v3, v4, starts, csr5,
+        tf, wt_te1_h, wt_te1_l, te_b1, wt_te2_h, wt_te2_l, te_b2, T, M0, NT, NPART);
+
+    buck_enc<<<NBUCK + MG, 256, 0, stream>>>(
+        bases, csr5, off5,
+        ef, wt_ee1_h, wt_ee1_l, ee_b1, wt_ee2_h, wt_ee2_l, ee_b2, Bf, M2, NT, NBUCK);
 
     #define LOFF(l) (off5 + (l) * (NT + 1))
     #define LCSR(l) (csr5 + (size_t)(l) * NE)
 
-    fused_mlp<64, true, true><<<2 * MG, 256, 0, stream>>>(
-        tf, wt_te1_h, wt_te1_l, te_b1, wt_te2_h, wt_te2_l, te_b2, T, M0,
-        ef, wt_ee1_h, wt_ee1_l, ee_b1, wt_ee2_h, wt_ee2_l, ee_b2, Bf, M2,
-        NT, MG);
-
-    gnn_fused<<<MG, 256, 0, stream>>>(
-        T, M0, LCSR(0), LOFF(0),
-        wt_g0_h, wt_g0_l, gb0, wt_g1_h, wt_g1_l, gb1, T, M1, NT);
+    gather_q_f8<<<GB, 256, 0, stream>>>(M0, LCSR(0), LOFF(0), T, S, F, 0.5f, NT);
+
+    fused_mlp<256><<<MG, 256, 0, stream>>>(
+        F, S, wt_g0_h, wt_g0_l, gb0, wt_g1_h, wt_g1_l, gb1, T, M1, NT, 0.5f);
+
+    gather_task2<<<GB, 256, 0, stream>>>(
+        M1, LCSR(1), LOFF(1), M2, LCSR(2), LOFF(2), T, S, M3, NT);
 
     gather_mean_f8<<<GB, 256, 0, stream>>>(
-        M1, LCSR(1), LOFF(1), T, F, M3,
-        M1, LCSR(1), LOFF(1), T, F, M3,
-        0.3f, GB, NT);
-
-    gather_mean_f8<<<2 * GB, 256, 0, stream>>>(
-        M2, LCSR(2), LOFF(2), F, S, nullptr,
-        M3, LCSR(3), LOFF(3), Bf, T, M4,
-        0.3f, GB, NT);
+        M3, LCSR(3), LOFF(3), Bf, F, M4, 0.3f, NT);
 
     gather_mean_f8<<<GB, 256, 0, stream>>>(
-        M4, LCSR(4), LOFF(4), T, Bf, nullptr,
-        M4, LCSR(4), LOFF(4), T, Bf, nullptr,
-        0.3f, GB, NT);
+        M4, LCSR(4), LOFF(4), F, Bf, nullptr, 0.3f, NT);
 
     colsum_slots<<<512, 256, 0, stream>>>(S, Bf, part, NT);
     final_mlp<<<1, 256, 0, stream>>>(part, 1.f / NT, 1.f / NEDGE,
```

Measured after the change: 434.5 us. -12.7%, faster.
